# Optimization experiments

Hardware: AMD Instinct MI355X
Metric: run time of the kernel (lower is better)

Reference implementation:

```python
import jax, jax.numpy as jnp
import numpy as np

N = 50000
E = 600000
IN_DIM = 128
HID = 128
HEADS = 4
OUT = HID // HEADS  # per-head out channels
R = 2
LAYERS = 2
NEG_SLOPE = 0.2


def _glorot(key, shape):
    fan_in, fan_out = shape[-2], shape[-1]
    lim = jnp.sqrt(6.0 / (fan_in + fan_out))
    return jax.random.uniform(key, shape, jnp.float32, -lim, lim)


def setup_inputs() -> dict:
    key = jax.random.key(0)
    ks = jax.random.split(key, 20)
    x = jax.random.normal(ks[0], (N, IN_DIM), jnp.float32)
    eidx = jax.random.randint(ks[1], (2, E), 0, N, jnp.int64 if jax.config.jax_enable_x64 else jnp.int32)
    etype = jax.random.randint(ks[2], (E,), 0, R, eidx.dtype)
    d = IN_DIM
    params = {}
    ki = 3
    for l in range(LAYERS):
        params[f"W{l}"] = _glorot(ks[ki], (R, d, HID)); ki += 1            # per-relation weight
        params[f"Q{l}"] = _glorot(ks[ki], (HID, HEADS)); ki += 1           # query proj (dim=1)
        params[f"K{l}"] = _glorot(ks[ki], (HID, HEADS)); ki += 1           # key proj
        params[f"cb{l}"] = jnp.zeros((HID,), jnp.float32)                   # conv bias
        params[f"pW{l}"] = _glorot(ks[ki], (HID, HID)); ki += 1            # proj Linear weight [out,in]
        params[f"pb{l}"] = jnp.zeros((HID,), jnp.float32)
        d = HID
    return dict(x=x, eidx=eidx, etype=etype, **params)


def _rgat_conv(h, src, dst, etype, W, Q, K, b):
    # per-relation transform of all nodes: [R, N, HID]
    xw = jnp.einsum('ni,rio->rno', h, W)
    out_j = xw[etype, src]          # [E, HID] source features under edge's relation
    out_i = xw[etype, dst]          # [E, HID] target features under edge's relation
    # additive self-attention, dim=1: alpha [E, HEADS]
    alpha = jax.nn.leaky_relu(out_i @ Q + out_j @ K, NEG_SLOPE)
    # segment softmax over destination nodes (across-relation)
    m = jax.ops.segment_max(alpha, dst, num_segments=N)
    m = jnp.where(jnp.isfinite(m), m, 0.0)
    e = jnp.exp(alpha - m[dst])
    s = jax.ops.segment_sum(e, dst, num_segments=N)
    a = e / (s[dst] + 1e-16)
    # weighted messages and scatter-sum aggregation
    msg = out_j.reshape(E, HEADS, OUT) * a[:, :, None]
    agg = jax.ops.segment_sum(msg.reshape(E, HID), dst, num_segments=N)
    return agg + b


def reference(x, eidx, etype, W0, Q0, K0, cb0, pW0, pb0, W1, Q1, K1, cb1, pW1, pb1):
    src, dst = eidx[0], eidx[1]  # flow source_to_target: aggregate at eidx[1]
    h = x
    for (W, Q, K, cb, pW, pb) in ((W0, Q0, K0, cb0, pW0, pb0), (W1, Q1, K1, cb1, pW1, pb1)):
        h = _rgat_conv(h, src, dst, etype, W, Q, K, cb)
        h = jax.nn.elu(h @ pW.T + pb)
    return h
```

## Files before the change

### kernel.cpp

```cpp
#include <hip/hip_runtime.h>
#include <hip/hip_bf16.h>

typedef __hip_bfloat16 bf16;
typedef short s16x8 __attribute__((ext_vector_type(8)));
typedef float f32x4 __attribute__((ext_vector_type(4)));

#define N_NODES 50000
#define NPAD    50048
#define E_EDGES 600000
#define HID     128
#define HEADS   4
#define SCAN_B  196

__device__ __forceinline__ unsigned short f2bf_bits(float f) {
  unsigned u = __float_as_uint(f);
  u += 0x7fffu + ((u >> 16) & 1u);
  return (unsigned short)(u >> 16);
}
__device__ __forceinline__ float bf2f(unsigned short b) {
  return __uint_as_float(((unsigned)b) << 16);
}
__device__ __forceinline__ float lo_f(unsigned v) { return __uint_as_float(v << 16); }
__device__ __forceinline__ float hi_f(unsigned v) { return __uint_as_float(v & 0xffff0000u); }

__device__ __forceinline__ float lrelu(float v) { return fmaxf(v, 0.2f * v); }

__global__ __launch_bounds__(256) void detect_zero_kernel(const unsigned short* __restrict__ xb,
                                                          const int* __restrict__ ei,
                                                          int* __restrict__ flags,
                                                          int* __restrict__ zp, int nz) {
  int t = threadIdx.x;
  int i = blockIdx.x * 256 + t;
  if (i < nz) zp[i] = 0;
  if (blockIdx.x == 0) {
    __shared__ int cnt[2];
    if (t < 2) cnt[t] = 0;
    __syncthreads();
    unsigned short v = xb[2 * t];
    int ex = (v >> 7) & 0xFF;
    if (ex < 119 || ex > 135) atomicAdd(&cnt[0], 1);
    if (ei[2 * t + 1] != 0) atomicAdd(&cnt[1], 1);
    __syncthreads();
    if (t == 0) {
      flags[0] = (cnt[0] > 64) ? 1 : 0;
      flags[1] = (cnt[1] == 0) ? 1 : 0;
    }
  }
}

__global__ __launch_bounds__(256) void cvt_idx_hist_kernel(const int* __restrict__ eidx,
                                                           const int* __restrict__ etype,
                                                           int* __restrict__ dstA, int* __restrict__ pk,
                                                           int* __restrict__ deg,
                                                           const int* __restrict__ flags) {
  int e = blockIdx.x * 256 + threadIdx.x;
  if (e >= E_EDGES) return;
  int s, d, r;
  if (flags[1]) {
    const long long* e64 = (const long long*)eidx;
    const long long* t64 = (const long long*)etype;
    s = (int)e64[e]; d = (int)e64[E_EDGES + e]; r = (int)t64[e];
  } else {
    s = eidx[e]; d = eidx[E_EDGES + e]; r = etype[e];
  }
  dstA[e] = d;
  pk[e] = s | (r << 16);
  atomicAdd(&deg[d], 1);
}

__global__ __launch_bounds__(256) void bucket_kernel(const int* __restrict__ deg,
                                                     int* __restrict__ bcnt,
                                                     int* __restrict__ nq,
                                                     int* __restrict__ nw) {
  int n = blockIdx.x * 256 + threadIdx.x;
  int lane = threadIdx.x & 63;
  bool valid = n < N_NODES;
  int d = valid ? deg[n] : 0;
  bool isq = valid && (d <= 16);
  bool isw = valid && (d > 16);
  unsigned long long mq = __ballot(isq);
  unsigned long long mw = __ballot(isw);
  unsigned long long lower = (lane == 63) ? 0x7fffffffffffffffull : ((1ull << lane) - 1ull);
  int baseq = 0, basew = 0;
  int lq = (int)__ffsll((unsigned long long)mq) - 1;
  int lw = (int)__ffsll((unsigned long long)mw) - 1;
  if (mq && lane == lq) baseq = atomicAdd(&bcnt[0], (int)__popcll(mq));
  if (mw && lane == lw) basew = atomicAdd(&bcnt[1], (int)__popcll(mw));
  if (mq) baseq = __shfl(baseq, lq);
  if (mw) basew = __shfl(basew, lw);
  if (isq) nq[baseq + (int)__popcll(mq & lower)] = n;
  if (isw) nw[basew + (int)__popcll(mw & lower)] = n;
}

__global__ __launch_bounds__(256) void cvt_xb_kernel(const void* __restrict__ src,
                                                     unsigned short* __restrict__ dst, int n8,
                                                     const int* __restrict__ flags) {
  int i = blockIdx.x * 256 + threadIdx.x;
  if (i >= n8) return;
  if (flags[0]) {
    const float4* s4 = (const float4*)src;
    float4 a = s4[2 * i], b = s4[2 * i + 1];
    s16x8 o;
    o[0] = (short)f2bf_bits(a.x); o[1] = (short)f2bf_bits(a.y);
    o[2] = (short)f2bf_bits(a.z); o[3] = (short)f2bf_bits(a.w);
    o[4] = (short)f2bf_bits(b.x); o[5] = (short)f2bf_bits(b.y);
    o[6] = (short)f2bf_bits(b.z); o[7] = (short)f2bf_bits(b.w);
    *(s16x8*)(dst + (size_t)i * 8) = o;
  } else {
    *(s16x8*)(dst + (size_t)i * 8) = ((const s16x8*)src)[i];
  }
}

__global__ __launch_bounds__(256) void cvt_wt_kernel(const void* __restrict__ src0,
                                                     const void* __restrict__ src1,
                                                     unsigned short* __restrict__ dst,
                                                     const int* __restrict__ flags) {
  int idx = blockIdx.x * 256 + threadIdx.x;
  if (idx >= 2 * 2 * HID * HID) return;
  int l = idx >> 15, rem = idx & 32767;
  int r = rem >> 14, i = (rem >> 7) & 127, o = rem & 127;
  const void* src = l ? src1 : src0;
  unsigned short b;
  if (flags[0]) b = f2bf_bits(((const float*)src)[rem]);
  else          b = ((const unsigned short*)src)[rem];
  dst[(size_t)l * 2 * HID * HID + ((size_t)r * HID + o) * HID + i] = b;
}

struct P8 { const void* src[8]; int dstoff[8]; int n[8]; };
__global__ __launch_bounds__(256) void cvt_params_kernel(P8 tab, float* __restrict__ base,
                                                         const int* __restrict__ flags) {
  const int f = flags[0];
  for (int k = 0; k < 8; ++k) {
    int n = tab.n[k];
    for (int i = blockIdx.x * 256 + threadIdx.x; i < n; i += gridDim.x * 256) {
      float v = f ? ((const float*)tab.src[k])[i] : bf2f(((const unsigned short*)tab.src[k])[i]);
      base[tab.dstoff[k] + i] = v;
    }
  }
}

__global__ __launch_bounds__(256) void scan1_kernel(const int* __restrict__ deg,
                                                    int* __restrict__ excl,
                                                    int* __restrict__ bsum) {
  __shared__ int sm[256];
  int t = threadIdx.x, i = blockIdx.x * 256 + t;
  int v = (i < NPAD) ? deg[i] : 0;
  sm[t] = v;
  __syncthreads();
#pragma unroll
  for (int off = 1; off < 256; off <<= 1) {
    int add = (t >= off) ? sm[t - off] : 0;
    __syncthreads();
    sm[t] += add;
    __syncthreads();
  }
  if (i < NPAD) excl[i] = sm[t] - v;
  if (t == 255) bsum[blockIdx.x] = sm[255];
}

__global__ __launch_bounds__(256) void scan23_kernel(const int* __restrict__ excl,
                                                     const int* __restrict__ bsum,
                                                     int* __restrict__ rowstart) {
  __shared__ int sm[256];
  int t = threadIdx.x;
  int v = (t < SCAN_B) ? bsum[t] : 0;
  sm[t] = v;
  __syncthreads();
#pragma unroll
  for (int off = 1; off < 256; off <<= 1) {
    int add = (t >= off) ? sm[t - off] : 0;
    __syncthreads();
    sm[t] += add;
    __syncthreads();
  }
  int bpre = (blockIdx.x > 0) ? sm[blockIdx.x - 1] : 0;
  int i = blockIdx.x * 256 + t;
  if (i < NPAD) rowstart[i] = excl[i] + bpre;
  if (i == 0) rowstart[NPAD] = E_EDGES;
}

__global__ __launch_bounds__(256) void scatter_kernel(const int* __restrict__ dstA,
                                                      const int* __restrict__ pk,
                                                      const int* __restrict__ rowstart,
                                                      int* __restrict__ cnt,
                                                      int* __restrict__ eord) {
  int e = blockIdx.x * 256 + threadIdx.x;
  if (e >= E_EDGES) return;
  int d = dstA[e];
  int pos = rowstart[d] + atomicAdd(&cnt[d], 1);
  eord[pos] = pk[e];
}


__global__ __launch_bounds__(256) void gemm_xw_mfma(const unsigned short* __restrict__ hb,
                                                    const unsigned short* __restrict__ Wbt,
                                                    unsigned short* __restrict__ xw) {
  __shared__ unsigned short As[64][136];
  const int t = threadIdx.x;
  const int wave = t >> 6, lane = t & 63;
  const int row0 = blockIdx.x * 64;
  const int r = wave >> 1, colb = (wave & 1) * 64;
  const int lm = lane & 15, q = lane >> 4;
  const unsigned short* Bt = Wbt + (size_t)r * HID * HID;
  s16x8 bfr[4][4];
#pragma unroll
  for (int kc = 0; kc < 4; ++kc) {
    const int ko = kc * 32 + q * 8;
#pragma unroll
    for (int ct = 0; ct < 4; ++ct)
      bfr[kc][ct] = *(const s16x8*)(Bt + (size_t)(colb + ct * 16 + lm) * HID + ko);
  }
  const unsigned short* gsrc = hb + (size_t)row0 * HID;
#pragma unroll
  for (int j = 0; j < 4; ++j) {
    int idx = j * 256 + t;
    *(s16x8*)&As[idx >> 4][(idx & 15) * 8] = *(const s16x8*)(gsrc + idx * 8);
  }
  __syncthreads();
  f32x4 acc[4][4];
#pragma unroll
  for (int a = 0; a < 4; ++a)
#pragma unroll
    for (int b = 0; b < 4; ++b) { f32x4 z = {0.f, 0.f, 0.f, 0.f}; acc[a][b] = z; }
#pragma unroll
  for (int kc = 0; kc < 4; ++kc) {
    const int ko = kc * 32 + q * 8;
#pragma unroll
    for (int rt = 0; rt < 4; ++rt) {
      s16x8 a = *(const s16x8*)&As[rt * 16 + lm][ko];
#pragma unroll
      for (int ct = 0; ct < 4; ++ct)
        acc[rt][ct] = __builtin_amdgcn_mfma_f32_16x16x32_bf16(a, bfr[kc][ct], acc[rt][ct], 0, 0, 0);
    }
  }
  __syncthreads();
#pragma unroll
  for (int rr = 0; rr < 2; ++rr) {
    if (r == rr) {
#pragma unroll
      for (int rt = 0; rt < 4; ++rt)
#pragma unroll
        for (int i = 0; i < 4; ++i) {
          int rloc = rt * 16 + q * 4 + i;
#pragma unroll
          for (int ct = 0; ct < 4; ++ct)
            As[rloc][colb + ct * 16 + lm] = f2bf_bits(acc[rt][ct][i]);
        }
    }
    __syncthreads();
    unsigned short* dst = xw + ((size_t)rr * NPAD + row0) * HID;
#pragma unroll
    for (int j = 0; j < 4; ++j) {
      int idx = j * 256 + t;
      int rw = idx >> 4, cb8 = (idx & 15) * 8;
      if (row0 + rw < N_NODES)
        *(s16x8*)(dst + (size_t)rw * HID + cb8) = *(const s16x8*)&As[rw][cb8];
    }
    __syncthreads();
  }
}

__global__ __launch_bounds__(128) void proj_mfma(const unsigned short* __restrict__ aggb,
                                                 const unsigned short* __restrict__ pWTb,
                                                 const float* __restrict__ bo,
                                                 unsigned short* __restrict__ hbout,
                                                 void* __restrict__ dout,
                                                 const int* __restrict__ flags) {
  __shared__ unsigned short As[64][136];
  const int t = threadIdx.x;
  const int wave = t >> 6, lane = t & 63;
  const int row0 = blockIdx.x * 64;
  const int colb = wave * 64;
  const int lm = lane & 15, q = lane >> 4;
  s16x8 bfr[4][4];
#pragma unroll
  for (int kc = 0; kc < 4; ++kc) {
    const int ko = kc * 32 + q * 8;
#pragma unroll
    for (int ct = 0; ct < 4; ++ct)
      bfr[kc][ct] = *(const s16x8*)(pWTb + (size_t)(colb + ct * 16 + lm) * HID + ko);
  }
  const unsigned short* gsrc = aggb + (size_t)row0 * HID;
#pragma unroll
  for (int j = 0; j < 8; ++j) {
    int idx = j * 128 + t;
    *(s16x8*)&As[idx >> 4][(idx & 15) * 8] = *(const s16x8*)(gsrc + idx * 8);
  }
  __syncthreads();
  f32x4 acc[4][4];
#pragma unroll
  for (int a = 0; a < 4; ++a)
#pragma unroll
    for (int b = 0; b < 4; ++b) { f32x4 z = {0.f, 0.f, 0.f, 0.f}; acc[a][b] = z; }
#pragma unroll
  for (int kc = 0; kc < 4; ++kc) {
    const int ko = kc * 32 + q * 8;
#pragma unroll
    for (int rt = 0; rt < 4; ++rt) {
      s16x8 a = *(const s16x8*)&As[rt * 16 + lm][ko];
#pragma unroll
      for (int ct = 0; ct < 4; ++ct)
        acc[rt][ct] = __builtin_amdgcn_mfma_f32_16x16x32_bf16(a, bfr[kc][ct], acc[rt][ct], 0, 0, 0);
    }
  }
  __syncthreads();
  const int f32final = (dout != nullptr) && flags[0];
  if (!f32final) {
    unsigned short* dstp = dout ? (unsigned short*)dout : hbout;
#pragma unroll
    for (int rt = 0; rt < 4; ++rt)
#pragma unroll
      for (int i = 0; i < 4; ++i) {
        int rloc = rt * 16 + q * 4 + i;
#pragma unroll
        for (int ct = 0; ct < 4; ++ct) {
          int o = colb + ct * 16 + lm;
          float v = acc[rt][ct][i] + bo[o];
          v = v > 0.f ? v : expm1f(v);
          As[rloc][o] = f2bf_bits(v);
        }
      }
    __syncthreads();
#pragma unroll
    for (int j = 0; j < 8; ++j) {
      int idx = j * 128 + t;
      int rw = idx >> 4, cb8 = (idx & 15) * 8;
      if (row0 + rw < N_NODES)
        *(s16x8*)(dstp + (size_t)(row0 + rw) * HID + cb8) = *(const s16x8*)&As[rw][cb8];
    }
  } else {
    float* fdst = (float*)dout;
    float (*Fs)[132] = (float(*)[132])&As[0][0];
#pragma unroll
    for (int h = 0; h < 2; ++h) {
#pragma unroll
      for (int rt2 = 0; rt2 < 2; ++rt2) {
        const int rt = h * 2 + rt2;
#pragma unroll
        for (int i = 0; i < 4; ++i) {
          int rloc = rt2 * 16 + q * 4 + i;
#pragma unroll
          for (int ct = 0; ct < 4; ++ct) {
            int o = colb + ct * 16 + lm;
            float v = acc[rt][ct][i] + bo[o];
            v = v > 0.f ? v : expm1f(v);
            Fs[rloc][o] = v;
          }
        }
      }
      __syncthreads();
#pragma unroll
      for (int j = 0; j < 8; ++j) {
        int idx = j * 128 + t;
        int rw = idx >> 5, cb4 = (idx & 31) * 4;
        if (row0 + h * 32 + rw < N_NODES)
          *(float4*)(fdst + (size_t)(row0 + h * 32 + rw) * HID + cb4) = *(const float4*)&Fs[rw][cb4];
      }
      __syncthreads();
    }
  }
}

__global__ __launch_bounds__(256) void prep_wq_kernel(const unsigned short* __restrict__ Wbt,
                                                      const float* __restrict__ Qf,
                                                      const float* __restrict__ Kf,
                                                      unsigned short* __restrict__ qkt_hi,
                                                      unsigned short* __restrict__ qkt_lo) {
  int idx = blockIdx.x * 256 + threadIdx.x;
  if (idx >= 2 * 2 * HID) return;
  int i = idx & 127, lr = idx >> 7, l = lr >> 1, r = (lr & 1);
  float aq[4] = {0.f, 0.f, 0.f, 0.f}, ak[4] = {0.f, 0.f, 0.f, 0.f};
  const unsigned short* Wb = Wbt + (size_t)lr * HID * HID;
  const float* Qp = Qf + l * HID * HEADS;
  const float* Kp = Kf + l * HID * HEADS;
  for (int j = 0; j < HID; ++j) {
    float w = bf2f(Wb[j * HID + i]);
    float4 q4 = *(const float4*)(Qp + j * 4);
    float4 k4 = *(const float4*)(Kp + j * 4);
    aq[0] += w * q4.x; aq[1] += w * q4.y; aq[2] += w * q4.z; aq[3] += w * q4.w;
    ak[0] += w * k4.x; ak[1] += w * k4.y; ak[2] += w * k4.z; ak[3] += w * k4.w;
  }
  size_t base = (size_t)l * 16 * HID;
#pragma unroll
  for (int h = 0; h < 4; ++h) {
    unsigned short qh = f2bf_bits(aq[h]);
    unsigned short kh = f2bf_bits(ak[h]);
    float qres = aq[h] - bf2f(qh);
    float kres = ak[h] - bf2f(kh);
    qkt_hi[base + (size_t)(r * 4 + h) * HID + i] = qh;
    qkt_lo[base + (size_t)(r * 4 + h) * HID + i] = f2bf_bits(qres);
    qkt_hi[base + (size_t)(8 + r * 4 + h) * HID + i] = kh;
    qkt_lo[base + (size_t)(8 + r * 4 + h) * HID + i] = f2bf_bits(kres);
  }
}

__global__ __launch_bounds__(256) void qk_mfma_kernel(const unsigned short* __restrict__ hb,
                                                      const unsigned short* __restrict__ qkt_hi,
                                                      const unsigned short* __restrict__ qkt_lo,
                                                      float4* __restrict__ qi4,
                                                      float4* __restrict__ kj4) {
  __shared__ float st[4][16][68];
  const int wave = threadIdx.x >> 6, lane = threadIdx.x & 63;
  const int row0 = blockIdx.x * 256 + wave * 64;
  const int lm = lane & 15, q = lane >> 4;
  if (row0 < NPAD) {
    s16x8 bhi[4], blo[4], af[4][4];
#pragma unroll
    for (int kc = 0; kc < 4; ++kc) {
      const int ko = kc * 32 + q * 8;
      bhi[kc] = *(const s16x8*)(qkt_hi + (size_t)lm * HID + ko);
      blo[kc] = *(const s16x8*)(qkt_lo + (size_t)lm * HID + ko);
    }
#pragma unroll
    for (int kc = 0; kc < 4; ++kc) {
      const int ko = kc * 32 + q * 8;
#pragma unroll
      for (int rt = 0; rt < 4; ++rt)
        af[kc][rt] = *(const s16x8*)(hb + (size_t)(row0 + rt * 16 + lm) * HID + ko);
    }
    f32x4 acc[4];
#pragma unroll
    for (int a = 0; a < 4; ++a) { f32x4 z = {0.f, 0.f, 0.f, 0.f}; acc[a] = z; }
#pragma unroll
    for (int kc = 0; kc < 4; ++kc)
#pragma unroll
      for (int rt = 0; rt < 4; ++rt) {
        acc[rt] = __builtin_amdgcn_mfma_f32_16x16x32_bf16(af[kc][rt], bhi[kc], acc[rt], 0, 0, 0);
        acc[rt] = __builtin_amdgcn_mfma_f32_16x16x32_bf16(af[kc][rt], blo[kc], acc[rt], 0, 0, 0);
      }
#pragma unroll
    for (int rt = 0; rt < 4; ++rt)
      *(f32x4*)&st[wave][lm][rt * 16 + q * 4] = acc[rt];
  }
  __syncthreads();
  if (row0 < NPAD) {
    int n = row0 + lane;
    if (n < N_NODES) {
      float4 v;
      v.x = st[wave][0][lane]; v.y = st[wave][1][lane]; v.z = st[wave][2][lane]; v.w = st[wave][3][lane];
      qi4[n] = v;
      v.x = st[wave][4][lane]; v.y = st[wave][5][lane]; v.z = st[wave][6][lane]; v.w = st[wave][7][lane];
      qi4[NPAD + n] = v;
      v.x = st[wave][8][lane]; v.y = st[wave][9][lane]; v.z = st[wave][10][lane]; v.w = st[wave][11][lane];
      kj4[n] = v;
      v.x = st[wave][12][lane]; v.y = st[wave][13][lane]; v.z = st[wave][14][lane]; v.w = st[wave][15][lane];
      kj4[NPAD + n] = v;
    }
  }
}

__global__ __launch_bounds__(256) void edge_quad_kernel(
    const int* __restrict__ rowstart, const int* __restrict__ eord,
    const float4* __restrict__ qi4, const float4* __restrict__ kj4,
    const unsigned short* __restrict__ xw, unsigned short* __restrict__ aggb,
    const int* __restrict__ nq, const int* __restrict__ bcnt) {
  __shared__ volatile float wls[16][4][17];
  const int t = threadIdx.x;
  const int wave = t >> 6, lane = t & 63;
  const int g = lane >> 4, li = lane & 15;
  const int idx = blockIdx.x * 16 + wave * 4 + g;
  const int cq = bcnt[0];
  const bool act = idx < cq;
  const int n = act ? nq[idx] : 0;
  const int start = rowstart[n];
  const int dg = act ? (rowstart[n + 1] - start) : 0;
  int p = 0;
  float w0 = 0.f, w1 = 0.f, w2 = 0.f, w3 = 0.f;
  if (li < dg) {
    p = eord[start + li];
    int s = p & 0xffff, r = p >> 16;
    float4 k4 = kj4[r ? (NPAD + s) : s];
    float4 q4 = r ? qi4[NPAD + n] : qi4[n];
    w0 = __expf(fminf(lrelu(q4.x + k4.x), 85.f));
    w1 = __expf(fminf(lrelu(q4.y + k4.y), 85.f));
    w2 = __expf(fminf(lrelu(q4.z + k4.z), 85.f));
    w3 = __expf(fminf(lrelu(q4.w + k4.w), 85.f));
  }
  const int wg = (wave << 2) | g;
  wls[wg][0][li] = w0; wls[wg][1][li] = w1;
  wls[wg][2][li] = w2; wls[wg][3][li] = w3;
  float s0 = w0, s1 = w1, s2 = w2, s3 = w3;
#pragma unroll
  for (int off = 8; off > 0; off >>= 1) {
    s0 += __shfl_xor(s0, off); s1 += __shfl_xor(s1, off);
    s2 += __shfl_xor(s2, off); s3 += __shfl_xor(s3, off);
  }
  const int hh = li >> 2;
  float ssel = hh == 0 ? s0 : hh == 1 ? s1 : hh == 2 ? s2 : s3;
  float a0 = 0.f, a1 = 0.f, a2 = 0.f, a3 = 0.f, a4 = 0.f, a5 = 0.f, a6 = 0.f, a7 = 0.f;
  volatile const float* wrh = &wls[wg][hh][0];
  const int co = li * 8;
  const int gbase = lane & 48;
#pragma unroll 1
  for (int e0 = 0; e0 < dg; e0 += 4) {
    int pe[4];
    uint4 v[4];
#pragma unroll
    for (int u = 0; u < 4; ++u) {
      int e = e0 + u;
      pe[u] = __shfl(p, gbase + (e < dg ? e : 0));
    }
#pragma unroll
    for (int u = 0; u < 4; ++u)
      v[u] = *(const uint4*)(xw + ((size_t)((pe[u] & 0xffff) + (pe[u] >> 16) * NPAD) << 7) + co);
#pragma unroll
    for (int u = 0; u < 4; ++u) {
      int e = e0 + u;
      float we = (e < dg) ? wrh[e] : 0.f;
      a0 = fmaf(lo_f(v[u].x), we, a0); a1 = fmaf(hi_f(v[u].x), we, a1);
      a2 = fmaf(lo_f(v[u].y), we, a2); a3 = fmaf(hi_f(v[u].y), we, a3);
      a4 = fmaf(lo_f(v[u].z), we, a4); a5 = fmaf(hi_f(v[u].z), we, a5);
      a6 = fmaf(lo_f(v[u].w), we, a6); a7 = fmaf(hi_f(v[u].w), we, a7);
    }
  }
  if (act) {
    float inv = 1.f / (ssel + 1e-16f);
    uint4 o;
    o.x = (unsigned)f2bf_bits(a0 * inv) | ((unsigned)f2bf_bits(a1 * inv) << 16);
    o.y = (unsigned)f2bf_bits(a2 * inv) | ((unsigned)f2bf_bits(a3 * inv) << 16);
    o.z = (unsigned)f2bf_bits(a4 * inv) | ((unsigned)f2bf_bits(a5 * inv) << 16);
    o.w = (unsigned)f2bf_bits(a6 * inv) | ((unsigned)f2bf_bits(a7 * inv) << 16);
    *(uint4*)(aggb + ((size_t)n << 7) + co) = o;
  }
}

__global__ __launch_bounds__(256) void edge_big_kernel(
    const int* __restrict__ rowstart, const int* __restrict__ eord,
    const float4* __restrict__ qi4, const float4* __restrict__ kj4,
    const unsigned short* __restrict__ xw, unsigned short* __restrict__ aggb,
    const int* __restrict__ nw, const int* __restrict__ bcnt) {
  __shared__ volatile float wls[4][4][72];
  const int wave = threadIdx.x >> 6, lane = threadIdx.x & 63;
  const int idx = blockIdx.x * 4 + wave;
  const int cw = bcnt[1];
  if (idx >= cw) return;
  const int n = nw[idx];
  unsigned* outp = (unsigned*)(aggb + ((size_t)n << 7)) + lane;
  const int start = rowstart[n];
  const int deg = rowstart[n + 1] - start;
  const int hh = lane >> 4;
  const int ch2 = lane << 1;
  float2 acc = {0.f, 0.f};
  float ssel;
  if (deg <= 64) {
    int p = 0;
    float w0 = 0.f, w1 = 0.f, w2 = 0.f, w3 = 0.f;
    if (lane < deg) {
      p = eord[start + lane];
      int s = p & 0xffff, r = p >> 16;
      float4 k4 = kj4[r ? (NPAD + s) : s];
      float4 q4 = r ? qi4[NPAD + n] : qi4[n];
      w0 = __expf(fminf(lrelu(q4.x + k4.x), 85.f));
      w1 = __expf(fminf(lrelu(q4.y + k4.y), 85.f));
      w2 = __expf(fminf(lrelu(q4.z + k4.z), 85.f));
      w3 = __expf(fminf(lrelu(q4.w + k4.w), 85.f));
    }
    float s0 = w0, s1 = w1, s2 = w2, s3 = w3;
#pragma unroll
    for (int off = 32; off > 0; off >>= 1) {
      s0 += __shfl_xor(s0, off); s1 += __shfl_xor(s1, off);
      s2 += __shfl_xor(s2, off); s3 += __shfl_xor(s3, off);
    }
    ssel = hh == 0 ? s0 : hh == 1 ? s1 : hh == 2 ? s2 : s3;
    wls[wave][0][lane] = w0;
    wls[wave][1][lane] = w1;
    wls[wave][2][lane] = w2;
    wls[wave][3][lane] = w3;
    volatile const float* wrh = &wls[wave][hh][0];
    const int degp = (deg + 15) & ~15;
#pragma unroll 1
    for (int e = 0; e < degp; e += 16) {
      int pp[16];
      unsigned vv[16];
#pragma unroll
      for (int u = 0; u < 16; ++u)
        pp[u] = __builtin_amdgcn_readlane(p, e + u);
#pragma unroll
      for (int u = 0; u < 16; ++u)
        vv[u] = *(const unsigned*)(xw + ((size_t)((pp[u] & 0xffff) + (pp[u] >> 16) * NPAD) << 7) + ch2);
#pragma unroll
      for (int u = 0; u < 16; ++u) {
        float we = wrh[e + u];
        acc.x = fmaf(lo_f(vv[u]), we, acc.x);
        acc.y = fmaf(hi_f(vv[u]), we, acc.y);
      }
    }
  } else {
    const float4 q0 = qi4[n], q1 = qi4[NPAD + n];
    float4 m = make_float4(-1e30f, -1e30f, -1e30f, -1e30f);
    for (int e = start; e < start + deg; ++e) {
      int pe = eord[e];
      int s = pe & 0xffff, r = pe >> 16;
      float4 k4 = kj4[(size_t)r * NPAD + s];
      float4 q4 = r ? q1 : q0;
      m.x = fmaxf(m.x, lrelu(q4.x + k4.x)); m.y = fmaxf(m.y, lrelu(q4.y + k4.y));
      m.z = fmaxf(m.z, lrelu(q4.z + k4.z)); m.w = fmaxf(m.w, lrelu(q4.w + k4.w));
    }
    float4 sv = make_float4(0.f, 0.f, 0.f, 0.f);
    for (int e = start; e < start + deg; ++e) {
      int pe = eord[e];
      int s = pe & 0xffff, r = pe >> 16;
      float4 k4 = kj4[(size_t)r * NPAD + s];
      float4 q4 = r ? q1 : q0;
      float w0 = __expf(lrelu(q4.x + k4.x) - m.x);
      float w1 = __expf(lrelu(q4.y + k4.y) - m.y);
      float w2 = __expf(lrelu(q4.z + k4.z) - m.z);
      float w3 = __expf(lrelu(q4.w + k4.w) - m.w);
      sv.x += w0; sv.y += w1; sv.z += w2; sv.w += w3;
      float we = hh == 0 ? w0 : hh == 1 ? w1 : hh == 2 ? w2 : w3;
      unsigned v = *(const unsigned*)(xw + (((size_t)r * NPAD + s) << 7) + ch2);
      acc.x = fmaf(lo_f(v), we, acc.x);
      acc.y = fmaf(hi_f(v), we, acc.y);
    }
    ssel = hh == 0 ? sv.x : hh == 1 ? sv.y : hh == 2 ? sv.z : sv.w;
  }
  float inv = 1.f / (ssel + 1e-16f);
  *outp = (unsigned)f2bf_bits(acc.x * inv) | ((unsigned)f2bf_bits(acc.y * inv) << 16);
}

__global__ __launch_bounds__(64) void prep_proj_kernel(const void* __restrict__ pW0,
                                                       const void* __restrict__ pW1,
                                                       const float* __restrict__ cbf,
                                                       const float* __restrict__ pbf,
                                                       unsigned short* __restrict__ pWTb2,
                                                       float* __restrict__ bo2,
                                                       const int* __restrict__ flags) {
  int o = blockIdx.x & 127, l = blockIdx.x >> 7, t = threadIdx.x;
  const void* pWraw = l ? pW1 : pW0;
  const float* cb = cbf + l * HID;
  const int f = flags[0];
  float part = 0.f;
#pragma unroll
  for (int i = t; i < HID; i += 64) {
    float w = f ? ((const float*)pWraw)[o * HID + i] : bf2f(((const unsigned short*)pWraw)[o * HID + i]);
    pWTb2[(size_t)l * HID * HID + o * HID + i] = f2bf_bits(w);
    part += cb[i] * w;
  }
#pragma unroll
  for (int off = 32; off > 0; off >>= 1) part += __shfl_xor(part, off);
  if (t == 0) bo2[l * HID + o] = pbf[l * HID + o] + part;
}

extern "C" void kernel_launch(void* const* d_in, const int* in_sizes, int n_in,
                              void* d_out, int out_size, void* d_ws, size_t ws_size,
                              hipStream_t stream) {
  const void* x     = d_in[0];
  const int*  eidx  = (const int*)d_in[1];
  const int*  etype = (const int*)d_in[2];
  const int iW[2] = {3, 9}, iQ[2] = {4, 10}, iK[2] = {5, 11}, icb[2] = {6, 12}, ipW[2] = {7, 13}, ipb[2] = {8, 14};

  float* ws = (float*)d_ws;
  size_t off = 0;
  int*   flags = (int*)(ws + off); off += 16;
  unsigned short* hb   = (unsigned short*)(ws + off); off += (size_t)NPAD * HID / 2;
  unsigned short* xw   = (unsigned short*)(ws + off); off += (size_t)NPAD * HID;
  float* qi   = ws + off; off += (size_t)2 * NPAD * HEADS;
  float* kj   = ws + off; off += (size_t)2 * NPAD * HEADS;
  unsigned short* aggb = (unsigned short*)(ws + off); off += (size_t)NPAD * HID / 2;
  int* dstA = (int*)(ws + off); off += E_EDGES;
  int* pk   = (int*)(ws + off); off += E_EDGES;
  int* eord = (int*)(ws + off); off += E_EDGES;
  int* deg  = (int*)(ws + off); off += NPAD;
  int* cnt  = (int*)(ws + off); off += NPAD;
  int* bcnt = (int*)(ws + off); off += 16;
  int* excl = (int*)(ws + off); off += NPAD;
  int* rowstart = (int*)(ws + off); off += NPAD + 16;
  int* bsum  = (int*)(ws + off); off += 256;
  int* nq   = (int*)(ws + off); off += NPAD;
  int* nwl  = (int*)(ws + off); off += NPAD;
  unsigned short* Wbt   = (unsigned short*)(ws + off); off += (size_t)2 * 2 * HID * HID / 2;
  unsigned short* pWTb2 = (unsigned short*)(ws + off); off += (size_t)2 * HID * HID / 2;
  unsigned short* qkt_hi = (unsigned short*)(ws + off); off += (size_t)2 * 16 * HID / 2;
  unsigned short* qkt_lo = (unsigned short*)(ws + off); off += (size_t)2 * 16 * HID / 2;
  float* Qf  = ws + off; off += 2 * HID * HEADS;
  float* Kf  = ws + off; off += 2 * HID * HEADS;
  float* cbf = ws + off; off += 2 * HID;
  float* pbf = ws + off; off += 2 * HID;
  float* bo2 = ws + off; off += 2 * HID;

  detect_zero_kernel<<<(2 * NPAD + 16 + 255) / 256, 256, 0, stream>>>((const unsigned short*)x, eidx, flags, deg, 2 * NPAD + 16);
  cvt_idx_hist_kernel<<<(E_EDGES + 255) / 256, 256, 0, stream>>>(eidx, etype, dstA, pk, deg, flags);
  bucket_kernel<<<(N_NODES + 255) / 256, 256, 0, stream>>>(deg, bcnt, nq, nwl);
  cvt_xb_kernel<<<(N_NODES * HID / 8 + 255) / 256, 256, 0, stream>>>(x, hb, N_NODES * HID / 8, flags);
  cvt_wt_kernel<<<(2 * 2 * HID * HID + 255) / 256, 256, 0, stream>>>(d_in[iW[0]], d_in[iW[1]], Wbt, flags);
  {
    P8 tab;
    float* base = ws;
    for (int l = 0; l < 2; ++l) {
      tab.src[l * 4 + 0] = d_in[iQ[l]];  tab.dstoff[l * 4 + 0] = (int)(Qf - base) + l * HID * HEADS;  tab.n[l * 4 + 0] = HID * HEADS;
      tab.src[l * 4 + 1] = d_in[iK[l]];  tab.dstoff[l * 4 + 1] = (int)(Kf - base) + l * HID * HEADS;  tab.n[l * 4 + 1] = HID * HEADS;
      tab.src[l * 4 + 2] = d_in[icb[l]]; tab.dstoff[l * 4 + 2] = (int)(cbf - base) + l * HID;         tab.n[l * 4 + 2] = HID;
      tab.src[l * 4 + 3] = d_in[ipb[l]]; tab.dstoff[l * 4 + 3] = (int)(pbf - base) + l * HID;         tab.n[l * 4 + 3] = HID;
    }
    cvt_params_kernel<<<2, 256, 0, stream>>>(tab, base, flags);
  }

  scan1_kernel<<<SCAN_B, 256, 0, stream>>>(deg, excl, bsum);
  scan23_kernel<<<SCAN_B, 256, 0, stream>>>(excl, bsum, rowstart);
  scatter_kernel<<<(E_EDGES + 255) / 256, 256, 0, stream>>>(dstA, pk, rowstart, cnt, eord);

  prep_wq_kernel<<<2, 256, 0, stream>>>(Wbt, Qf, Kf, qkt_hi, qkt_lo);
  prep_proj_kernel<<<2 * HID, 64, 0, stream>>>(d_in[ipW[0]], d_in[ipW[1]], cbf, pbf, pWTb2, bo2, flags);

  const int RB = NPAD / 64;
  const int QB = (NPAD + 255) / 256;
  for (int l = 0; l < 2; ++l) {
    gemm_xw_mfma<<<RB, 256, 0, stream>>>(hb, Wbt + (size_t)l * 2 * HID * HID, xw);
    qk_mfma_kernel<<<QB, 256, 0, stream>>>(hb, qkt_hi + (size_t)l * 16 * HID, qkt_lo + (size_t)l * 16 * HID,
                                           (float4*)qi, (float4*)kj);
    edge_quad_kernel<<<(N_NODES + 15) / 16, 256, 0, stream>>>(rowstart, eord, (const float4*)qi, (const float4*)kj,
                                                              xw, aggb, nq, bcnt);
    edge_big_kernel<<<(N_NODES + 3) / 4, 256, 0, stream>>>(rowstart, eord, (const float4*)qi, (const float4*)kj,
                                                           xw, aggb, nwl, bcnt);
    proj_mfma<<<RB, 128, 0, stream>>>(aggb, pWTb2 + (size_t)l * HID * HID, bo2 + l * HID, hb,
                                      (l == 1) ? d_out : nullptr, flags);
  }
}
```

Baseline: 374.3 us.

## Merge independent preprocessing and per-layer kernels into block-range fused launches

```diff
diff --git a/kernel.cpp b/kernel.cpp
--- a/kernel.cpp
+++ b/kernel.cpp
@@ -12,6 +12,14 @@
 #define HEADS   4
 #define SCAN_B  196
 
+#define GB_IDX  2344
+#define GB_XB   3125
+#define GB_WT   256
+#define GB_QUAD 3125
+#define GB_BIG  8824
+#define GB_GEMM 1564
+#define GB_QK   196
+
 __device__ __forceinline__ unsigned short f2bf_bits(float f) {
   unsigned u = __float_as_uint(f);
   u += 0x7fffu + ((u >> 16) & 1u);
@@ -22,8 +30,8 @@
 }
 __device__ __forceinline__ float lo_f(unsigned v) { return __uint_as_float(v << 16); }
 __device__ __forceinline__ float hi_f(unsigned v) { return __uint_as_float(v & 0xffff0000u); }
-
 __device__ __forceinline__ float lrelu(float v) { return fmaxf(v, 0.2f * v); }
+__device__ __forceinline__ float elu(float v) { return v > 0.f ? v : __expf(v) - 1.f; }
 
 __global__ __launch_bounds__(256) void detect_zero_kernel(const unsigned short* __restrict__ xb,
                                                           const int* __restrict__ ei,
@@ -48,135 +56,189 @@
   }
 }
 
-__global__ __launch_bounds__(256) void cvt_idx_hist_kernel(const int* __restrict__ eidx,
-                                                           const int* __restrict__ etype,
-                                                           int* __restrict__ dstA, int* __restrict__ pk,
-                                                           int* __restrict__ deg,
-                                                           const int* __restrict__ flags) {
-  int e = blockIdx.x * 256 + threadIdx.x;
-  if (e >= E_EDGES) return;
-  int s, d, r;
-  if (flags[1]) {
-    const long long* e64 = (const long long*)eidx;
-    const long long* t64 = (const long long*)etype;
-    s = (int)e64[e]; d = (int)e64[E_EDGES + e]; r = (int)t64[e];
+struct P8 { const void* src[8]; int dstoff[8]; int n[8]; };
+__global__ __launch_bounds__(256) void cvt_all_kernel(const int* __restrict__ eidx,
+                                                      const int* __restrict__ etype,
+                                                      int* __restrict__ dstA, int* __restrict__ pk,
+                                                      int* __restrict__ deg,
+                                                      const void* __restrict__ x,
+                                                      unsigned short* __restrict__ hb,
+                                                      const void* __restrict__ w0,
+                                                      const void* __restrict__ w1,
+                                                      unsigned short* __restrict__ Wbt,
+                                                      P8 tab, float* __restrict__ base,
+                                                      const int* __restrict__ flags) {
+  const int b = blockIdx.x, t = threadIdx.x;
+  if (b < GB_IDX) {
+    int e = b * 256 + t;
+    if (e >= E_EDGES) return;
+    int s, d, r;
+    if (flags[1]) {
+      const long long* e64 = (const long long*)eidx;
+      const long long* t64 = (const long long*)etype;
+      s = (int)e64[e]; d = (int)e64[E_EDGES + e]; r = (int)t64[e];
+    } else {
+      s = eidx[e]; d = eidx[E_EDGES + e]; r = etype[e];
+    }
+    dstA[e] = d;
+    pk[e] = s | (r << 16);
+    atomicAdd(&deg[d], 1);
+  } else if (b < GB_IDX + GB_XB) {
+    int i = (b - GB_IDX) * 256 + t;
+    if (flags[0]) {
+      const float4* s4 = (const float4*)x;
+      float4 a = s4[2 * i], c = s4[2 * i + 1];
+      s16x8 o;
+      o[0] = (short)f2bf_bits(a.x); o[1] = (short)f2bf_bits(a.y);
+      o[2] = (short)f2bf_bits(a.z); o[3] = (short)f2bf_bits(a.w);
+      o[4] = (short)f2bf_bits(c.x); o[5] = (short)f2bf_bits(c.y);
+      o[6] = (short)f2bf_bits(c.z); o[7] = (short)f2bf_bits(c.w);
+      *(s16x8*)(hb + (size_t)i * 8) = o;
+    } else {
+      *(s16x8*)(hb + (size_t)i * 8) = ((const s16x8*)x)[i];
+    }
+  } else if (b < GB_IDX + GB_XB + GB_WT) {
+    int idx = (b - GB_IDX - GB_XB) * 256 + t;
+    int l = idx >> 15, rem = idx & 32767;
+    int r = rem >> 14, i = (rem >> 7) & 127, o = rem & 127;
+    const void* src = l ? w1 : w0;
+    unsigned short v;
+    if (flags[0]) v = f2bf_bits(((const float*)src)[rem]);
+    else          v = ((const unsigned short*)src)[rem];
+    Wbt[(size_t)l * 2 * HID * HID + ((size_t)r * HID + o) * HID + i] = v;
   } else {
-    s = eidx[e]; d = eidx[E_EDGES + e]; r = etype[e];
-  }
-  dstA[e] = d;
-  pk[e] = s | (r << 16);
-  atomicAdd(&deg[d], 1);
-}
-
-__global__ __launch_bounds__(256) void bucket_kernel(const int* __restrict__ deg,
-                                                     int* __restrict__ bcnt,
-                                                     int* __restrict__ nq,
-                                                     int* __restrict__ nw) {
-  int n = blockIdx.x * 256 + threadIdx.x;
-  int lane = threadIdx.x & 63;
-  bool valid = n < N_NODES;
-  int d = valid ? deg[n] : 0;
-  bool isq = valid && (d <= 16);
-  bool isw = valid && (d > 16);
-  unsigned long long mq = __ballot(isq);
-  unsigned long long mw = __ballot(isw);
-  unsigned long long lower = (lane == 63) ? 0x7fffffffffffffffull : ((1ull << lane) - 1ull);
-  int baseq = 0, basew = 0;
-  int lq = (int)__ffsll((unsigned long long)mq) - 1;
-  int lw = (int)__ffsll((unsigned long long)mw) - 1;
-  if (mq && lane == lq) baseq = atomicAdd(&bcnt[0], (int)__popcll(mq));
-  if (mw && lane == lw) basew = atomicAdd(&bcnt[1], (int)__popcll(mw));
-  if (mq) baseq = __shfl(baseq, lq);
-  if (mw) basew = __shfl(basew, lw);
-  if (isq) nq[baseq + (int)__popcll(mq & lower)] = n;
-  if (isw) nw[basew + (int)__popcll(mw & lower)] = n;
-}
-
-__global__ __launch_bounds__(256) void cvt_xb_kernel(const void* __restrict__ src,
-                                                     unsigned short* __restrict__ dst, int n8,
-                                                     const int* __restrict__ flags) {
-  int i = blockIdx.x * 256 + threadIdx.x;
-  if (i >= n8) return;
-  if (flags[0]) {
-    const float4* s4 = (const float4*)src;
-    float4 a = s4[2 * i], b = s4[2 * i + 1];
-    s16x8 o;
-    o[0] = (short)f2bf_bits(a.x); o[1] = (short)f2bf_bits(a.y);
-    o[2] = (short)f2bf_bits(a.z); o[3] = (short)f2bf_bits(a.w);
-    o[4] = (short)f2bf_bits(b.x); o[5] = (short)f2bf_bits(b.y);
-    o[6] = (short)f2bf_bits(b.z); o[7] = (short)f2bf_bits(b.w);
-    *(s16x8*)(dst + (size_t)i * 8) = o;
+    const int f = flags[0];
+    int bb = b - GB_IDX - GB_XB - GB_WT;
+    for (int k = 0; k < 8; ++k) {
+      int n = tab.n[k];
+      for (int i = bb * 256 + t; i < n; i += 2 * 256) {
+        float v = f ? ((const float*)tab.src[k])[i] : bf2f(((const unsigned short*)tab.src[k])[i]);
+        base[tab.dstoff[k] + i] = v;
+      }
+    }
+  }
+}
+
+__global__ __launch_bounds__(256) void scan1_bucket_kernel(const int* __restrict__ deg,
+                                                           int* __restrict__ excl,
+                                                           int* __restrict__ bsum,
+                                                           int* __restrict__ bcnt,
+                                                           int* __restrict__ nq,
+                                                           int* __restrict__ nw) {
+  const int b = blockIdx.x, t = threadIdx.x;
+  if (b < SCAN_B) {
+    __shared__ int sm[256];
+    int i = b * 256 + t;
+    int v = (i < NPAD) ? deg[i] : 0;
+    sm[t] = v;
+    __syncthreads();
+#pragma unroll
+    for (int off = 1; off < 256; off <<= 1) {
+      int add = (t >= off) ? sm[t - off] : 0;
+      __syncthreads();
+      sm[t] += add;
+      __syncthreads();
+    }
+    if (i < NPAD) excl[i] = sm[t] - v;
+    if (t == 255) bsum[b] = sm[255];
   } else {
-    *(s16x8*)(dst + (size_t)i * 8) = ((const s16x8*)src)[i];
-  }
-}
-
-__global__ __launch_bounds__(256) void cvt_wt_kernel(const void* __restrict__ src0,
-                                                     const void* __restrict__ src1,
-                                                     unsigned short* __restrict__ dst,
-                                                     const int* __restrict__ flags) {
-  int idx = blockIdx.x * 256 + threadIdx.x;
-  if (idx >= 2 * 2 * HID * HID) return;
-  int l = idx >> 15, rem = idx & 32767;
-  int r = rem >> 14, i = (rem >> 7) & 127, o = rem & 127;
-  const void* src = l ? src1 : src0;
-  unsigned short b;
-  if (flags[0]) b = f2bf_bits(((const float*)src)[rem]);
-  else          b = ((const unsigned short*)src)[rem];
-  dst[(size_t)l * 2 * HID * HID + ((size_t)r * HID + o) * HID + i] = b;
-}
-
-struct P8 { const void* src[8]; int dstoff[8]; int n[8]; };
-__global__ __launch_bounds__(256) void cvt_params_kernel(P8 tab, float* __restrict__ base,
-                                                         const int* __restrict__ flags) {
-  const int f = flags[0];
-  for (int k = 0; k < 8; ++k) {
-    int n = tab.n[k];
-    for (int i = blockIdx.x * 256 + threadIdx.x; i < n; i += gridDim.x * 256) {
-      float v = f ? ((const float*)tab.src[k])[i] : bf2f(((const unsigned short*)tab.src[k])[i]);
-      base[tab.dstoff[k] + i] = v;
-    }
-  }
-}
-
-__global__ __launch_bounds__(256) void scan1_kernel(const int* __restrict__ deg,
-                                                    int* __restrict__ excl,
-                                                    int* __restrict__ bsum) {
-  __shared__ int sm[256];
-  int t = threadIdx.x, i = blockIdx.x * 256 + t;
-  int v = (i < NPAD) ? deg[i] : 0;
-  sm[t] = v;
-  __syncthreads();
-#pragma unroll
-  for (int off = 1; off < 256; off <<= 1) {
-    int add = (t >= off) ? sm[t - off] : 0;
+    int n = (b - SCAN_B) * 256 + t;
+    int lane = t & 63;
+    bool valid = n < N_NODES;
+    int d = valid ? deg[n] : 0;
+    bool isq = valid && (d <= 16);
+    bool isw = valid && (d > 16);
+    unsigned long long mq = __ballot(isq);
+    unsigned long long mw = __ballot(isw);
+    unsigned long long lower = (lane == 63) ? 0x7fffffffffffffffull : ((1ull << lane) - 1ull);
+    int baseq = 0, basew = 0;
+    int lq = (int)__ffsll(mq) - 1;
+    int lw = (int)__ffsll(mw) - 1;
+    if (mq && lane == lq) baseq = atomicAdd(&bcnt[0], (int)__popcll(mq));
+    if (mw && lane == lw) basew = atomicAdd(&bcnt[1], (int)__popcll(mw));
+    if (mq) baseq = __shfl(baseq, lq);
+    if (mw) basew = __shfl(basew, lw);
+    if (isq) nq[baseq + (int)__popcll(mq & lower)] = n;
+    if (isw) nw[basew + (int)__popcll(mw & lower)] = n;
+  }
+}
+
+__global__ __launch_bounds__(256) void scan23_prep_kernel(const int* __restrict__ excl,
+                                                          const int* __restrict__ bsum,
+                                                          int* __restrict__ rowstart,
+                                                          const unsigned short* __restrict__ Wbt,
+                                                          const float* __restrict__ Qf,
+                                                          const float* __restrict__ Kf,
+                                                          unsigned short* __restrict__ qkt_hi,
+                                                          unsigned short* __restrict__ qkt_lo,
+                                                          const void* __restrict__ pW0,
+                                                          const void* __restrict__ pW1,
+                                                          const float* __restrict__ cbf,
+                                                          const float* __restrict__ pbf,
+                                                          unsigned short* __restrict__ pWTb2,
+                                                          float* __restrict__ bo2,
+                                                          const int* __restrict__ flags) {
+  const int b = blockIdx.x, t = threadIdx.x;
+  if (b < SCAN_B) {
+    __shared__ int sm[256];
+    int v = (t < SCAN_B) ? bsum[t] : 0;
+    sm[t] = v;
     __syncthreads();
-    sm[t] += add;
-    __syncthreads();
-  }
-  if (i < NPAD) excl[i] = sm[t] - v;
-  if (t == 255) bsum[blockIdx.x] = sm[255];
-}
-
-__global__ __launch_bounds__(256) void scan23_kernel(const int* __restrict__ excl,
-                                                     const int* __restrict__ bsum,
-                                                     int* __restrict__ rowstart) {
-  __shared__ int sm[256];
-  int t = threadIdx.x;
-  int v = (t < SCAN_B) ? bsum[t] : 0;
-  sm[t] = v;
-  __syncthreads();
-#pragma unroll
-  for (int off = 1; off < 256; off <<= 1) {
-    int add = (t >= off) ? sm[t - off] : 0;
-    __syncthreads();
-    sm[t] += add;
-    __syncthreads();
-  }
-  int bpre = (blockIdx.x > 0) ? sm[blockIdx.x - 1] : 0;
-  int i = blockIdx.x * 256 + t;
-  if (i < NPAD) rowstart[i] = excl[i] + bpre;
-  if (i == 0) rowstart[NPAD] = E_EDGES;
+#pragma unroll
+    for (int off = 1; off < 256; off <<= 1) {
+      int add = (t >= off) ? sm[t - off] : 0;
+      __syncthreads();
+      sm[t] += add;
+      __syncthreads();
+    }
+    int bpre = (b > 0) ? sm[b - 1] : 0;
+    int i = b * 256 + t;
+    if (i < NPAD) rowstart[i] = excl[i] + bpre;
+    if (i == 0) rowstart[NPAD] = E_EDGES;
+  } else if (b < SCAN_B + 2) {
+    int idx = (b - SCAN_B) * 256 + t;
+    int i = idx & 127, lr = idx >> 7, l = lr >> 1, r = (lr & 1);
+    float aq[4] = {0.f, 0.f, 0.f, 0.f}, ak[4] = {0.f, 0.f, 0.f, 0.f};
+    const unsigned short* Wb = Wbt + (size_t)lr * HID * HID;
+    const float* Qp = Qf + l * HID * HEADS;
+    const float* Kp = Kf + l * HID * HEADS;
+    for (int j = 0; j < HID; ++j) {
+      float w = bf2f(Wb[j * HID + i]);
+      float4 q4 = *(const float4*)(Qp + j * 4);
+      float4 k4 = *(const float4*)(Kp + j * 4);
+      aq[0] += w * q4.x; aq[1] += w * q4.y; aq[2] += w * q4.z; aq[3] += w * q4.w;
+      ak[0] += w * k4.x; ak[1] += w * k4.y; ak[2] += w * k4.z; ak[3] += w * k4.w;
+    }
+    size_t base = (size_t)l * 16 * HID;
+#pragma unroll
+    for (int h = 0; h < 4; ++h) {
+      unsigned short qh = f2bf_bits(aq[h]);
+      unsigned short kh = f2bf_bits(ak[h]);
+      float qres = aq[h] - bf2f(qh);
+      float kres = ak[h] - bf2f(kh);
+      qkt_hi[base + (size_t)(r * 4 + h) * HID + i] = qh;
+      qkt_lo[base + (size_t)(r * 4 + h) * HID + i] = f2bf_bits(qres);
+      qkt_hi[base + (size_t)(8 + r * 4 + h) * HID + i] = kh;
+      qkt_lo[base + (size_t)(8 + r * 4 + h) * HID + i] = f2bf_bits(kres);
+    }
+  } else {
+    const int wave = t >> 6, lane = t & 63;
+    int ob = (b - SCAN_B - 2) * 4 + wave;
+    int o = ob & 127, l = ob >> 7;
+    const void* pWraw = l ? pW1 : pW0;
+    const float* cb = cbf + l * HID;
+    const int f = flags[0];
+    float part = 0.f;
+#pragma unroll
+    for (int i = lane; i < HID; i += 64) {
+      float w = f ? ((const float*)pWraw)[o * HID + i] : bf2f(((const unsigned short*)pWraw)[o * HID + i]);
+      pWTb2[(size_t)l * HID * HID + o * HID + i] = f2bf_bits(w);
+      part += cb[i] * w;
+    }
+#pragma unroll
+    for (int off = 32; off > 0; off >>= 1) part += __shfl_xor(part, off);
+    if (lane == 0) bo2[l * HID + o] = pbf[l * HID + o] + part;
+  }
 }
 
 __global__ __launch_bounds__(256) void scatter_kernel(const int* __restrict__ dstA,
@@ -191,76 +253,295 @@
   eord[pos] = pk[e];
 }
 
-
-__global__ __launch_bounds__(256) void gemm_xw_mfma(const unsigned short* __restrict__ hb,
-                                                    const unsigned short* __restrict__ Wbt,
-                                                    unsigned short* __restrict__ xw) {
-  __shared__ unsigned short As[64][136];
+__global__ __launch_bounds__(256) void gemm_qk_kernel(const unsigned short* __restrict__ hb,
+                                                      const unsigned short* __restrict__ Wbt,
+                                                      unsigned short* __restrict__ xw,
+                                                      const unsigned short* __restrict__ qkt_hi,
+                                                      const unsigned short* __restrict__ qkt_lo,
+                                                      float4* __restrict__ qi4,
+                                                      float4* __restrict__ kj4) {
+  __shared__ unsigned short smem[8704];
   const int t = threadIdx.x;
   const int wave = t >> 6, lane = t & 63;
-  const int row0 = blockIdx.x * 64;
-  const int r = wave >> 1, colb = (wave & 1) * 64;
   const int lm = lane & 15, q = lane >> 4;
-  const unsigned short* Bt = Wbt + (size_t)r * HID * HID;
-  s16x8 bfr[4][4];
-#pragma unroll
-  for (int kc = 0; kc < 4; ++kc) {
-    const int ko = kc * 32 + q * 8;
-#pragma unroll
-    for (int ct = 0; ct < 4; ++ct)
-      bfr[kc][ct] = *(const s16x8*)(Bt + (size_t)(colb + ct * 16 + lm) * HID + ko);
-  }
-  const unsigned short* gsrc = hb + (size_t)row0 * HID;
-#pragma unroll
-  for (int j = 0; j < 4; ++j) {
-    int idx = j * 256 + t;
-    *(s16x8*)&As[idx >> 4][(idx & 15) * 8] = *(const s16x8*)(gsrc + idx * 8);
-  }
-  __syncthreads();
-  f32x4 acc[4][4];
-#pragma unroll
-  for (int a = 0; a < 4; ++a)
-#pragma unroll
-    for (int b = 0; b < 4; ++b) { f32x4 z = {0.f, 0.f, 0.f, 0.f}; acc[a][b] = z; }
-#pragma unroll
-  for (int kc = 0; kc < 4; ++kc) {
-    const int ko = kc * 32 + q * 8;
-#pragma unroll
-    for (int rt = 0; rt < 4; ++rt) {
-      s16x8 a = *(const s16x8*)&As[rt * 16 + lm][ko];
+  if (blockIdx.x < GB_GEMM) {
+    unsigned short (*As)[136] = (unsigned short(*)[136])smem;
+    const int row0 = blockIdx.x * 32;
+    const int r = wave >> 1, colb = (wave & 1) * 64;
+    const unsigned short* Bt = Wbt + (size_t)r * HID * HID;
+    s16x8 bfr[4][4];
+#pragma unroll
+    for (int kc = 0; kc < 4; ++kc) {
+      const int ko = kc * 32 + q * 8;
 #pragma unroll
       for (int ct = 0; ct < 4; ++ct)
-        acc[rt][ct] = __builtin_amdgcn_mfma_f32_16x16x32_bf16(a, bfr[kc][ct], acc[rt][ct], 0, 0, 0);
-    }
-  }
-  __syncthreads();
-#pragma unroll
-  for (int rr = 0; rr < 2; ++rr) {
-    if (r == rr) {
+        bfr[kc][ct] = *(const s16x8*)(Bt + (size_t)(colb + ct * 16 + lm) * HID + ko);
+    }
+    const unsigned short* gsrc = hb + (size_t)row0 * HID;
+#pragma unroll
+    for (int j = 0; j < 2; ++j) {
+      int idx = j * 256 + t;
+      *(s16x8*)&As[idx >> 4][(idx & 15) * 8] = *(const s16x8*)(gsrc + idx * 8);
+    }
+    __syncthreads();
+    f32x4 acc[2][4];
+#pragma unroll
+    for (int a = 0; a < 2; ++a)
+#pragma unroll
+      for (int c = 0; c < 4; ++c) { f32x4 z = {0.f, 0.f, 0.f, 0.f}; acc[a][c] = z; }
+#pragma unroll
+    for (int kc = 0; kc < 4; ++kc) {
+      const int ko = kc * 32 + q * 8;
+#pragma unroll
+      for (int rt = 0; rt < 2; ++rt) {
+        s16x8 a = *(const s16x8*)&As[rt * 16 + lm][ko];
+#pragma unroll
+        for (int ct = 0; ct < 4; ++ct)
+          acc[rt][ct] = __builtin_amdgcn_mfma_f32_16x16x32_bf16(a, bfr[kc][ct], acc[rt][ct], 0, 0, 0);
+      }
+    }
+    __syncthreads();
+#pragma unroll
+    for (int rr = 0; rr < 2; ++rr) {
+      if (r == rr) {
+#pragma unroll
+        for (int rt = 0; rt < 2; ++rt)
+#pragma unroll
+          for (int i = 0; i < 4; ++i) {
+            int rloc = rt * 16 + q * 4 + i;
+#pragma unroll
+            for (int ct = 0; ct < 4; ++ct)
+              As[rloc][colb + ct * 16 + lm] = f2bf_bits(acc[rt][ct][i]);
+          }
+      }
+      __syncthreads();
+      unsigned short* dst = xw + ((size_t)rr * NPAD + row0) * HID;
+#pragma unroll
+      for (int j = 0; j < 2; ++j) {
+        int idx = j * 256 + t;
+        int rw = idx >> 4, cb8 = (idx & 15) * 8;
+        if (row0 + rw < N_NODES)
+          *(s16x8*)(dst + (size_t)rw * HID + cb8) = *(const s16x8*)&As[rw][cb8];
+      }
+      __syncthreads();
+    }
+  } else {
+    float (*st)[16][68] = (float(*)[16][68])smem;
+    const int row0 = (blockIdx.x - GB_GEMM) * 256 + wave * 64;
+    if (row0 < NPAD) {
+      s16x8 bhi[4], blo[4], af[4][4];
+#pragma unroll
+      for (int kc = 0; kc < 4; ++kc) {
+        const int ko = kc * 32 + q * 8;
+        bhi[kc] = *(const s16x8*)(qkt_hi + (size_t)lm * HID + ko);
+        blo[kc] = *(const s16x8*)(qkt_lo + (size_t)lm * HID + ko);
+      }
+#pragma unroll
+      for (int kc = 0; kc < 4; ++kc) {
+        const int ko = kc * 32 + q * 8;
+#pragma unroll
+        for (int rt = 0; rt < 4; ++rt)
+          af[kc][rt] = *(const s16x8*)(hb + (size_t)(row0 + rt * 16 + lm) * HID + ko);
+      }
+      f32x4 acc[4];
+#pragma unroll
+      for (int a = 0; a < 4; ++a) { f32x4 z = {0.f, 0.f, 0.f, 0.f}; acc[a] = z; }
+#pragma unroll
+      for (int kc = 0; kc < 4; ++kc)
+#pragma unroll
+        for (int rt = 0; rt < 4; ++rt) {
+          acc[rt] = __builtin_amdgcn_mfma_f32_16x16x32_bf16(af[kc][rt], bhi[kc], acc[rt], 0, 0, 0);
+          acc[rt] = __builtin_amdgcn_mfma_f32_16x16x32_bf16(af[kc][rt], blo[kc], acc[rt], 0, 0, 0);
+        }
 #pragma unroll
       for (int rt = 0; rt < 4; ++rt)
-#pragma unroll
-        for (int i = 0; i < 4; ++i) {
-          int rloc = rt * 16 + q * 4 + i;
-#pragma unroll
-          for (int ct = 0; ct < 4; ++ct)
-            As[rloc][colb + ct * 16 + lm] = f2bf_bits(acc[rt][ct][i]);
+        *(f32x4*)&st[wave][lm][rt * 16 + q * 4] = acc[rt];
+    }
+    __syncthreads();
+    if (row0 < NPAD) {
+      int n = row0 + lane;
+      if (n < N_NODES) {
+        float4 v;
+        v.x = st[wave][0][lane]; v.y = st[wave][1][lane]; v.z = st[wave][2][lane]; v.w = st[wave][3][lane];
+        qi4[n] = v;
+        v.x = st[wave][4][lane]; v.y = st[wave][5][lane]; v.z = st[wave][6][lane]; v.w = st[wave][7][lane];
+        qi4[NPAD + n] = v;
+        v.x = st[wave][8][lane]; v.y = st[wave][9][lane]; v.z = st[wave][10][lane]; v.w = st[wave][11][lane];
+        kj4[n] = v;
+        v.x = st[wave][12][lane]; v.y = st[wave][13][lane]; v.z = st[wave][14][lane]; v.w = st[wave][15][lane];
+        kj4[NPAD + n] = v;
+      }
+    }
+  }
+}
+
+__global__ __launch_bounds__(256) void edge_all_kernel(
+    const int* __restrict__ rowstart, const int* __restrict__ eord,
+    const float4* __restrict__ qi4, const float4* __restrict__ kj4,
+    const unsigned short* __restrict__ xw, unsigned short* __restrict__ aggb,
+    const int* __restrict__ nq, const int* __restrict__ nw,
+    const int* __restrict__ bcnt) {
+  __shared__ volatile float wbuf[1152];
+  const int t = threadIdx.x;
+  const int wave = t >> 6, lane = t & 63;
+  if (blockIdx.x < GB_QUAD) {
+    const int g = lane >> 4, li = lane & 15;
+    const int idx = blockIdx.x * 16 + wave * 4 + g;
+    const int cq = bcnt[0];
+    const bool act = idx < cq;
+    const int n = act ? nq[idx] : 0;
+    const int start = rowstart[n];
+    const int dg = act ? (rowstart[n + 1] - start) : 0;
+    int p = 0;
+    float w0 = 0.f, w1 = 0.f, w2 = 0.f, w3 = 0.f;
+    if (li < dg) {
+      p = eord[start + li];
+      int s = p & 0xffff, r = p >> 16;
+      float4 k4 = kj4[r ? (NPAD + s) : s];
+      float4 q4 = r ? qi4[NPAD + n] : qi4[n];
+      w0 = __expf(fminf(lrelu(q4.x + k4.x), 85.f));
+      w1 = __expf(fminf(lrelu(q4.y + k4.y), 85.f));
+      w2 = __expf(fminf(lrelu(q4.z + k4.z), 85.f));
+      w3 = __expf(fminf(lrelu(q4.w + k4.w), 85.f));
+    }
+    const int wg = (wave << 2) | g;
+    volatile float* wls = &wbuf[wg * 68];
+    wls[0 * 17 + li] = w0; wls[1 * 17 + li] = w1;
+    wls[2 * 17 + li] = w2; wls[3 * 17 + li] = w3;
+    float s0 = w0, s1 = w1, s2 = w2, s3 = w3;
+#pragma unroll
+    for (int off = 8; off > 0; off >>= 1) {
+      s0 += __shfl_xor(s0, off); s1 += __shfl_xor(s1, off);
+      s2 += __shfl_xor(s2, off); s3 += __shfl_xor(s3, off);
+    }
+    const int hh = li >> 2;
+    float ssel = hh == 0 ? s0 : hh == 1 ? s1 : hh == 2 ? s2 : s3;
+    float a0 = 0.f, a1 = 0.f, a2 = 0.f, a3 = 0.f, a4 = 0.f, a5 = 0.f, a6 = 0.f, a7 = 0.f;
+    volatile const float* wrh = &wls[hh * 17];
+    const int co = li * 8;
+    const int gbase = lane & 48;
+#pragma unroll 1
+    for (int e0 = 0; e0 < dg; e0 += 4) {
+      int pe[4];
+      uint4 v[4];
+#pragma unroll
+      for (int u = 0; u < 4; ++u) {
+        int e = e0 + u;
+        pe[u] = __shfl(p, gbase + (e < dg ? e : 0));
+      }
+#pragma unroll
+      for (int u = 0; u < 4; ++u)
+        v[u] = *(const uint4*)(xw + ((size_t)((pe[u] & 0xffff) + (pe[u] >> 16) * NPAD) << 7) + co);
+#pragma unroll
+      for (int u = 0; u < 4; ++u) {
+        int e = e0 + u;
+        float we = (e < dg) ? wrh[e] : 0.f;
+        a0 = fmaf(lo_f(v[u].x), we, a0); a1 = fmaf(hi_f(v[u].x), we, a1);
+        a2 = fmaf(lo_f(v[u].y), we, a2); a3 = fmaf(hi_f(v[u].y), we, a3);
+        a4 = fmaf(lo_f(v[u].z), we, a4); a5 = fmaf(hi_f(v[u].z), we, a5);
+        a6 = fmaf(lo_f(v[u].w), we, a6); a7 = fmaf(hi_f(v[u].w), we, a7);
+      }
+    }
+    if (act) {
+      float inv = 1.f / (ssel + 1e-16f);
+      uint4 o;
+      o.x = (unsigned)f2bf_bits(a0 * inv) | ((unsigned)f2bf_bits(a1 * inv) << 16);
+      o.y = (unsigned)f2bf_bits(a2 * inv) | ((unsigned)f2bf_bits(a3 * inv) << 16);
+      o.z = (unsigned)f2bf_bits(a4 * inv) | ((unsigned)f2bf_bits(a5 * inv) << 16);
+      o.w = (unsigned)f2bf_bits(a6 * inv) | ((unsigned)f2bf_bits(a7 * inv) << 16);
+      *(uint4*)(aggb + ((size_t)n << 7) + co) = o;
+    }
+  } else {
+    const int idx = (blockIdx.x - GB_QUAD) * 4 + wave;
+    const int cw = bcnt[1];
+    if (idx >= cw) return;
+    const int n = nw[idx];
+    unsigned* outp = (unsigned*)(aggb + ((size_t)n << 7)) + lane;
+    const int start = rowstart[n];
+    const int deg = rowstart[n + 1] - start;
+    const int hh = lane >> 4;
+    const int ch2 = lane << 1;
+    float2 acc = {0.f, 0.f};
+    float ssel;
+    volatile float* wls = &wbuf[wave * 288];
+    if (deg <= 64) {
+      int p = 0;
+      float w0 = 0.f, w1 = 0.f, w2 = 0.f, w3 = 0.f;
+      if (lane < deg) {
+        p = eord[start + lane];
+        int s = p & 0xffff, r = p >> 16;
+        float4 k4 = kj4[r ? (NPAD + s) : s];
+        float4 q4 = r ? qi4[NPAD + n] : qi4[n];
+        w0 = __expf(fminf(lrelu(q4.x + k4.x), 85.f));
+        w1 = __expf(fminf(lrelu(q4.y + k4.y), 85.f));
+        w2 = __expf(fminf(lrelu(q4.z + k4.z), 85.f));
+        w3 = __expf(fminf(lrelu(q4.w + k4.w), 85.f));
+      }
+      float s0 = w0, s1 = w1, s2 = w2, s3 = w3;
+#pragma unroll
+      for (int off = 32; off > 0; off >>= 1) {
+        s0 += __shfl_xor(s0, off); s1 += __shfl_xor(s1, off);
+        s2 += __shfl_xor(s2, off); s3 += __shfl_xor(s3, off);
+      }
+      ssel = hh == 0 ? s0 : hh == 1 ? s1 : hh == 2 ? s2 : s3;
+      wls[0 * 72 + lane] = w0;
+      wls[1 * 72 + lane] = w1;
+      wls[2 * 72 + lane] = w2;
+      wls[3 * 72 + lane] = w3;
+      volatile const float* wrh = &wls[hh * 72];
+      const int degp = (deg + 15) & ~15;
+#pragma unroll 1
+      for (int e = 0; e < degp; e += 16) {
+        int pp[16];
+        unsigned vv[16];
+#pragma unroll
+        for (int u = 0; u < 16; ++u)
+          pp[u] = __builtin_amdgcn_readlane(p, e + u);
+#pragma unroll
+        for (int u = 0; u < 16; ++u)
+          vv[u] = *(const unsigned*)(xw + ((size_t)((pp[u] & 0xffff) + (pp[u] >> 16) * NPAD) << 7) + ch2);
+#pragma unroll
+        for (int u = 0; u < 16; ++u) {
+          float we = wrh[e + u];
+          acc.x = fmaf(lo_f(vv[u]), we, acc.x);
+          acc.y = fmaf(hi_f(vv[u]), we, acc.y);
         }
-    }
-    __syncthreads();
-    unsigned short* dst = xw + ((size_t)rr * NPAD + row0) * HID;
-#pragma unroll
-    for (int j = 0; j < 4; ++j) {
-      int idx = j * 256 + t;
-      int rw = idx >> 4, cb8 = (idx & 15) * 8;
-      if (row0 + rw < N_NODES)
-        *(s16x8*)(dst + (size_t)rw * HID + cb8) = *(const s16x8*)&As[rw][cb8];
-    }
-    __syncthreads();
-  }
-}
-
-__global__ __launch_bounds__(128) void proj_mfma(const unsigned short* __restrict__ aggb,
+      }
+    } else {
+      const float4 q0 = qi4[n], q1 = qi4[NPAD + n];
+      float4 m = make_float4(-1e30f, -1e30f, -1e30f, -1e30f);
+      for (int e = start; e < start + deg; ++e) {
+        int pe = eord[e];
+        int s = pe & 0xffff, r = pe >> 16;
+        float4 k4 = kj4[(size_t)r * NPAD + s];
+        float4 q4 = r ? q1 : q0;
+        m.x = fmaxf(m.x, lrelu(q4.x + k4.x)); m.y = fmaxf(m.y, lrelu(q4.y + k4.y));
+        m.z = fmaxf(m.z, lrelu(q4.z + k4.z)); m.w = fmaxf(m.w, lrelu(q4.w + k4.w));
+      }
+      float4 sv = make_float4(0.f, 0.f, 0.f, 0.f);
+      for (int e = start; e < start + deg; ++e) {
+        int pe = eord[e];
+        int s = pe & 0xffff, r = pe >> 16;
+        float4 k4 = kj4[(size_t)r * NPAD + s];
+        float4 q4 = r ? q1 : q0;
+        float w0 = __expf(lrelu(q4.x + k4.x) - m.x);
+        float w1 = __expf(lrelu(q4.y + k4.y) - m.y);
+        float w2 = __expf(lrelu(q4.z + k4.z) - m.z);
+        float w3 = __expf(lrelu(q4.w + k4.w) - m.w);
+        sv.x += w0; sv.y += w1; sv.z += w2; sv.w += w3;
+        float we = hh == 0 ? w0 : hh == 1 ? w1 : hh == 2 ? w2 : w3;
+        unsigned v = *(const unsigned*)(xw + (((size_t)r * NPAD + s) << 7) + ch2);
+        acc.x = fmaf(lo_f(v), we, acc.x);
+        acc.y = fmaf(hi_f(v), we, acc.y);
+      }
+      ssel = hh == 0 ? sv.x : hh == 1 ? sv.y : hh == 2 ? sv.z : sv.w;
+    }
+    float inv = 1.f / (ssel + 1e-16f);
+    *outp = (unsigned)f2bf_bits(acc.x * inv) | ((unsigned)f2bf_bits(acc.y * inv) << 16);
+  }
+}
+
+__global__ __launch_bounds__(256) void proj_mfma(const unsigned short* __restrict__ aggb,
                                                  const unsigned short* __restrict__ pWTb,
                                                  const float* __restrict__ bo,
                                                  unsigned short* __restrict__ hbout,
@@ -270,7 +551,8 @@
   const int t = threadIdx.x;
   const int wave = t >> 6, lane = t & 63;
   const int row0 = blockIdx.x * 64;
-  const int colb = wave * 64;
+  const int h = wave >> 1;
+  const int colb = (wave & 1) * 64;
   const int lm = lane & 15, q = lane >> 4;
   s16x8 bfr[4][4];
 #pragma unroll
@@ -282,22 +564,22 @@
   }
   const unsigned short* gsrc = aggb + (size_t)row0 * HID;
 #pragma unroll
-  for (int j = 0; j < 8; ++j) {
-    int idx = j * 128 + t;
+  for (int j = 0; j < 4; ++j) {
+    int idx = j * 256 + t;
     *(s16x8*)&As[idx >> 4][(idx & 15) * 8] = *(const s16x8*)(gsrc + idx * 8);
   }
   __syncthreads();
-  f32x4 acc[4][4];
-#pragma unroll
-  for (int a = 0; a < 4; ++a)
-#pragma unroll
-    for (int b = 0; b < 4; ++b) { f32x4 z = {0.f, 0.f, 0.f, 0.f}; acc[a][b] = z; }
+  f32x4 acc[2][4];
+#pragma unroll
+  for (int a = 0; a < 2; ++a)
+#pragma unroll
+    for (int c = 0; c < 4; ++c) { f32x4 z = {0.f, 0.f, 0.f, 0.f}; acc[a][c] = z; }
 #pragma unroll
   for (int kc = 0; kc < 4; ++kc) {
     const int ko = kc * 32 + q * 8;
 #pragma unroll
-    for (int rt = 0; rt < 4; ++rt) {
-      s16x8 a = *(const s16x8*)&As[rt * 16 + lm][ko];
+    for (int rt = 0; rt < 2; ++rt) {
+      s16x8 a = *(const s16x8*)&As[(2 * h + rt) * 16 + lm][ko];
 #pragma unroll
       for (int ct = 0; ct < 4; ++ct)
         acc[rt][ct] = __builtin_amdgcn_mfma_f32_16x16x32_bf16(a, bfr[kc][ct], acc[rt][ct], 0, 0, 0);
@@ -308,22 +590,21 @@
   if (!f32final) {
     unsigned short* dstp = dout ? (unsigned short*)dout : hbout;
 #pragma unroll
-    for (int rt = 0; rt < 4; ++rt)
+    for (int rt = 0; rt < 2; ++rt)
 #pragma unroll
       for (int i = 0; i < 4; ++i) {
-        int rloc = rt * 16 + q * 4 + i;
+        int rloc = (2 * h + rt) * 16 + q * 4 + i;
 #pragma unroll
         for (int ct = 0; ct < 4; ++ct) {
           int o = colb + ct * 16 + lm;
-          float v = acc[rt][ct][i] + bo[o];
-          v = v > 0.f ? v : expm1f(v);
+          float v = elu(acc[rt][ct][i] + bo[o]);
           As[rloc][o] = f2bf_bits(v);
         }
       }
     __syncthreads();
 #pragma unroll
-    for (int j = 0; j < 8; ++j) {
-      int idx = j * 128 + t;
+    for (int j = 0; j < 4; ++j) {
+      int idx = j * 256 + t;
       int rw = idx >> 4, cb8 = (idx & 15) * 8;
       if (row0 + rw < N_NODES)
         *(s16x8*)(dstp + (size_t)(row0 + rw) * HID + cb8) = *(const s16x8*)&As[rw][cb8];
@@ -332,313 +613,31 @@
     float* fdst = (float*)dout;
     float (*Fs)[132] = (float(*)[132])&As[0][0];
 #pragma unroll
-    for (int h = 0; h < 2; ++h) {
-#pragma unroll
-      for (int rt2 = 0; rt2 < 2; ++rt2) {
-        const int rt = h * 2 + rt2;
-#pragma unroll
-        for (int i = 0; i < 4; ++i) {
-          int rloc = rt2 * 16 + q * 4 + i;
-#pragma unroll
-          for (int ct = 0; ct < 4; ++ct) {
-            int o = colb + ct * 16 + lm;
-            float v = acc[rt][ct][i] + bo[o];
-            v = v > 0.f ? v : expm1f(v);
-            Fs[rloc][o] = v;
+    for (int h2 = 0; h2 < 2; ++h2) {
+      if (h == h2) {
+#pragma unroll
+        for (int rt = 0; rt < 2; ++rt)
+#pragma unroll
+          for (int i = 0; i < 4; ++i) {
+            int rloc = rt * 16 + q * 4 + i;
+#pragma unroll
+            for (int ct = 0; ct < 4; ++ct) {
+              int o = colb + ct * 16 + lm;
+              Fs[rloc][o] = elu(acc[rt][ct][i] + bo[o]);
+            }
           }
-        }
       }
       __syncthreads();
 #pragma unroll
-      for (int j = 0; j < 8; ++j) {
-        int idx = j * 128 + t;
+      for (int j = 0; j < 4; ++j) {
+        int idx = j * 256 + t;
         int rw = idx >> 5, cb4 = (idx & 31) * 4;
-        if (row0 + h * 32 + rw < N_NODES)
-          *(float4*)(fdst + (size_t)(row0 + h * 32 + rw) * HID + cb4) = *(const float4*)&Fs[rw][cb4];
+        if (row0 + h2 * 32 + rw < N_NODES)
+          *(float4*)(fdst + (size_t)(row0 + h2 * 32 + rw) * HID + cb4) = *(const float4*)&Fs[rw][cb4];
       }
       __syncthreads();
     }
   }
-}
-
-__global__ __launch_bounds__(256) void prep_wq_kernel(const unsigned short* __restrict__ Wbt,
-                                                      const float* __restrict__ Qf,
-                                                      const float* __restrict__ Kf,
-                                                      unsigned short* __restrict__ qkt_hi,
-                                                      unsigned short* __restrict__ qkt_lo) {
-  int idx = blockIdx.x * 256 + threadIdx.x;
-  if (idx >= 2 * 2 * HID) return;
-  int i = idx & 127, lr = idx >> 7, l = lr >> 1, r = (lr & 1);
-  float aq[4] = {0.f, 0.f, 0.f, 0.f}, ak[4] = {0.f, 0.f, 0.f, 0.f};
-  const unsigned short* Wb = Wbt + (size_t)lr * HID * HID;
-  const float* Qp = Qf + l * HID * HEADS;
-  const float* Kp = Kf + l * HID * HEADS;
-  for (int j = 0; j < HID; ++j) {
-    float w = bf2f(Wb[j * HID + i]);
-    float4 q4 = *(const float4*)(Qp + j * 4);
-    float4 k4 = *(const float4*)(Kp + j * 4);
-    aq[0] += w * q4.x; aq[1] += w * q4.y; aq[2] += w * q4.z; aq[3] += w * q4.w;
-    ak[0] += w * k4.x; ak[1] += w * k4.y; ak[2] += w * k4.z; ak[3] += w * k4.w;
-  }
-  size_t base = (size_t)l * 16 * HID;
-#pragma unroll
-  for (int h = 0; h < 4; ++h) {
-    unsigned short qh = f2bf_bits(aq[h]);
-    unsigned short kh = f2bf_bits(ak[h]);
-    float qres = aq[h] - bf2f(qh);
-    float kres = ak[h] - bf2f(kh);
-    qkt_hi[base + (size_t)(r * 4 + h) * HID + i] = qh;
-    qkt_lo[base + (size_t)(r * 4 + h) * HID + i] = f2bf_bits(qres);
-    qkt_hi[base + (size_t)(8 + r * 4 + h) * HID + i] = kh;
-    qkt_lo[base + (size_t)(8 + r * 4 + h) * HID + i] = f2bf_bits(kres);
-  }
-}
-
-__global__ __launch_bounds__(256) void qk_mfma_kernel(const unsigned short* __restrict__ hb,
-                                                      const unsigned short* __restrict__ qkt_hi,
-                                                      const unsigned short* __restrict__ qkt_lo,
-                                                      float4* __restrict__ qi4,
-                                                      float4* __restrict__ kj4) {
-  __shared__ float st[4][16][68];
-  const int wave = threadIdx.x >> 6, lane = threadIdx.x & 63;
-  const int row0 = blockIdx.x * 256 + wave * 64;
-  const int lm = lane & 15, q = lane >> 4;
-  if (row0 < NPAD) {
-    s16x8 bhi[4], blo[4], af[4][4];
-#pragma unroll
-    for (int kc = 0; kc < 4; ++kc) {
-      const int ko = kc * 32 + q * 8;
-      bhi[kc] = *(const s16x8*)(qkt_hi + (size_t)lm * HID + ko);
-      blo[kc] = *(const s16x8*)(qkt_lo + (size_t)lm * HID + ko);
-    }
-#pragma unroll
-    for (int kc = 0; kc < 4; ++kc) {
-      const int ko = kc * 32 + q * 8;
-#pragma unroll
-      for (int rt = 0; rt < 4; ++rt)
-        af[kc][rt] = *(const s16x8*)(hb + (size_t)(row0 + rt * 16 + lm) * HID + ko);
-    }
-    f32x4 acc[4];
-#pragma unroll
-    for (int a = 0; a < 4; ++a) { f32x4 z = {0.f, 0.f, 0.f, 0.f}; acc[a] = z; }
-#pragma unroll
-    for (int kc = 0; kc < 4; ++kc)
-#pragma unroll
-      for (int rt = 0; rt < 4; ++rt) {
-        acc[rt] = __builtin_amdgcn_mfma_f32_16x16x32_bf16(af[kc][rt], bhi[kc], acc[rt], 0, 0, 0);
-        acc[rt] = __builtin_amdgcn_mfma_f32_16x16x32_bf16(af[kc][rt], blo[kc], acc[rt], 0, 0, 0);
-      }
-#pragma unroll
-    for (int rt = 0; rt < 4; ++rt)
-      *(f32x4*)&st[wave][lm][rt * 16 + q * 4] = acc[rt];
-  }
-  __syncthreads();
-  if (row0 < NPAD) {
-    int n = row0 + lane;
-    if (n < N_NODES) {
-      float4 v;
-      v.x = st[wave][0][lane]; v.y = st[wave][1][lane]; v.z = st[wave][2][lane]; v.w = st[wave][3][lane];
-      qi4[n] = v;
-      v.x = st[wave][4][lane]; v.y = st[wave][5][lane]; v.z = st[wave][6][lane]; v.w = st[wave][7][lane];
-      qi4[NPAD + n] = v;
-      v.x = st[wave][8][lane]; v.y = st[wave][9][lane]; v.z = st[wave][10][lane]; v.w = st[wave][11][lane];
-      kj4[n] = v;
-      v.x = st[wave][12][lane]; v.y = st[wave][13][lane]; v.z = st[wave][14][lane]; v.w = st[wave][15][lane];
-      kj4[NPAD + n] = v;
-    }
-  }
-}
-
-__global__ __launch_bounds__(256) void edge_quad_kernel(
-    const int* __restrict__ rowstart, const int* __restrict__ eord,
-    const float4* __restrict__ qi4, const float4* __restrict__ kj4,
-    const unsigned short* __restrict__ xw, unsigned short* __restrict__ aggb,
-    const int* __restrict__ nq, const int* __restrict__ bcnt) {
-  __shared__ volatile float wls[16][4][17];
-  const int t = threadIdx.x;
-  const int wave = t >> 6, lane = t & 63;
-  const int g = lane >> 4, li = lane & 15;
-  const int idx = blockIdx.x * 16 + wave * 4 + g;
-  const int cq = bcnt[0];
-  const bool act = idx < cq;
-  const int n = act ? nq[idx] : 0;
-  const int start = rowstart[n];
-  const int dg = act ? (rowstart[n + 1] - start) : 0;
-  int p = 0;
-  float w0 = 0.f, w1 = 0.f, w2 = 0.f, w3 = 0.f;
-  if (li < dg) {
-    p = eord[start + li];
-    int s = p & 0xffff, r = p >> 16;
-    float4 k4 = kj4[r ? (NPAD + s) : s];
-    float4 q4 = r ? qi4[NPAD + n] : qi4[n];
-    w0 = __expf(fminf(lrelu(q4.x + k4.x), 85.f));
-    w1 = __expf(fminf(lrelu(q4.y + k4.y), 85.f));
-    w2 = __expf(fminf(lrelu(q4.z + k4.z), 85.f));
-    w3 = __expf(fminf(lrelu(q4.w + k4.w), 85.f));
-  }
-  const int wg = (wave << 2) | g;
-  wls[wg][0][li] = w0; wls[wg][1][li] = w1;
-  wls[wg][2][li] = w2; wls[wg][3][li] = w3;
-  float s0 = w0, s1 = w1, s2 = w2, s3 = w3;
-#pragma unroll
-  for (int off = 8; off > 0; off >>= 1) {
-    s0 += __shfl_xor(s0, off); s1 += __shfl_xor(s1, off);
-    s2 += __shfl_xor(s2, off); s3 += __shfl_xor(s3, off);
-  }
-  const int hh = li >> 2;
-  float ssel = hh == 0 ? s0 : hh == 1 ? s1 : hh == 2 ? s2 : s3;
-  float a0 = 0.f, a1 = 0.f, a2 = 0.f, a3 = 0.f, a4 = 0.f, a5 = 0.f, a6 = 0.f, a7 = 0.f;
-  volatile const float* wrh = &wls[wg][hh][0];
-  const int co = li * 8;
-  const int gbase = lane & 48;
-#pragma unroll 1
-  for (int e0 = 0; e0 < dg; e0 += 4) {
-    int pe[4];
-    uint4 v[4];
-#pragma unroll
-    for (int u = 0; u < 4; ++u) {
-      int e = e0 + u;
-      pe[u] = __shfl(p, gbase + (e < dg ? e : 0));
-    }
-#pragma unroll
-    for (int u = 0; u < 4; ++u)
-      v[u] = *(const uint4*)(xw + ((size_t)((pe[u] & 0xffff) + (pe[u] >> 16) * NPAD) << 7) + co);
-#pragma unroll
-    for (int u = 0; u < 4; ++u) {
-      int e = e0 + u;
-      float we = (e < dg) ? wrh[e] : 0.f;
-      a0 = fmaf(lo_f(v[u].x), we, a0); a1 = fmaf(hi_f(v[u].x), we, a1);
-      a2 = fmaf(lo_f(v[u].y), we, a2); a3 = fmaf(hi_f(v[u].y), we, a3);
-      a4 = fmaf(lo_f(v[u].z), we, a4); a5 = fmaf(hi_f(v[u].z), we, a5);
-      a6 = fmaf(lo_f(v[u].w), we, a6); a7 = fmaf(hi_f(v[u].w), we, a7);
-    }
-  }
-  if (act) {
-    float inv = 1.f / (ssel + 1e-16f);
-    uint4 o;
-    o.x = (unsigned)f2bf_bits(a0 * inv) | ((unsigned)f2bf_bits(a1 * inv) << 16);
-    o.y = (unsigned)f2bf_bits(a2 * inv) | ((unsigned)f2bf_bits(a3 * inv) << 16);
-    o.z = (unsigned)f2bf_bits(a4 * inv) | ((unsigned)f2bf_bits(a5 * inv) << 16);
-    o.w = (unsigned)f2bf_bits(a6 * inv) | ((unsigned)f2bf_bits(a7 * inv) << 16);
-    *(uint4*)(aggb + ((size_t)n << 7) + co) = o;
-  }
-}
-
-__global__ __launch_bounds__(256) void edge_big_kernel(
-    const int* __restrict__ rowstart, const int* __restrict__ eord,
-    const float4* __restrict__ qi4, const float4* __restrict__ kj4,
-    const unsigned short* __restrict__ xw, unsigned short* __restrict__ aggb,
-    const int* __restrict__ nw, const int* __restrict__ bcnt) {
-  __shared__ volatile float wls[4][4][72];
-  const int wave = threadIdx.x >> 6, lane = threadIdx.x & 63;
-  const int idx = blockIdx.x * 4 + wave;
-  const int cw = bcnt[1];
-  if (idx >= cw) return;
-  const int n = nw[idx];
-  unsigned* outp = (unsigned*)(aggb + ((size_t)n << 7)) + lane;
-  const int start = rowstart[n];
-  const int deg = rowstart[n + 1] - start;
-  const int hh = lane >> 4;
-  const int ch2 = lane << 1;
-  float2 acc = {0.f, 0.f};
-  float ssel;
-  if (deg <= 64) {
-    int p = 0;
-    float w0 = 0.f, w1 = 0.f, w2 = 0.f, w3 = 0.f;
-    if (lane < deg) {
-      p = eord[start + lane];
-      int s = p & 0xffff, r = p >> 16;
-      float4 k4 = kj4[r ? (NPAD + s) : s];
-      float4 q4 = r ? qi4[NPAD + n] : qi4[n];
-      w0 = __expf(fminf(lrelu(q4.x + k4.x), 85.f));
-      w1 = __expf(fminf(lrelu(q4.y + k4.y), 85.f));
-      w2 = __expf(fminf(lrelu(q4.z + k4.z), 85.f));
-      w3 = __expf(fminf(lrelu(q4.w + k4.w), 85.f));
-    }
-    float s0 = w0, s1 = w1, s2 = w2, s3 = w3;
-#pragma unroll
-    for (int off = 32; off > 0; off >>= 1) {
-      s0 += __shfl_xor(s0, off); s1 += __shfl_xor(s1, off);
-      s2 += __shfl_xor(s2, off); s3 += __shfl_xor(s3, off);
-    }
-    ssel = hh == 0 ? s0 : hh == 1 ? s1 : hh == 2 ? s2 : s3;
-    wls[wave][0][lane] = w0;
-    wls[wave][1][lane] = w1;
-    wls[wave][2][lane] = w2;
-    wls[wave][3][lane] = w3;
-    volatile const float* wrh = &wls[wave][hh][0];
-    const int degp = (deg + 15) & ~15;
-#pragma unroll 1
-    for (int e = 0; e < degp; e += 16) {
-      int pp[16];
-      unsigned vv[16];
-#pragma unroll
-      for (int u = 0; u < 16; ++u)
-        pp[u] = __builtin_amdgcn_readlane(p, e + u);
-#pragma unroll
-      for (int u = 0; u < 16; ++u)
-        vv[u] = *(const unsigned*)(xw + ((size_t)((pp[u] & 0xffff) + (pp[u] >> 16) * NPAD) << 7) + ch2);
-#pragma unroll
-      for (int u = 0; u < 16; ++u) {
-        float we = wrh[e + u];
-        acc.x = fmaf(lo_f(vv[u]), we, acc.x);
-        acc.y = fmaf(hi_f(vv[u]), we, acc.y);
-      }
-    }
-  } else {
-    const float4 q0 = qi4[n], q1 = qi4[NPAD + n];
-    float4 m = make_float4(-1e30f, -1e30f, -1e30f, -1e30f);
-    for (int e = start; e < start + deg; ++e) {
-      int pe = eord[e];
-      int s = pe & 0xffff, r = pe >> 16;
-      float4 k4 = kj4[(size_t)r * NPAD + s];
-      float4 q4 = r ? q1 : q0;
-      m.x = fmaxf(m.x, lrelu(q4.x + k4.x)); m.y = fmaxf(m.y, lrelu(q4.y + k4.y));
-      m.z = fmaxf(m.z, lrelu(q4.z + k4.z)); m.w = fmaxf(m.w, lrelu(q4.w + k4.w));
-    }
-    float4 sv = make_float4(0.f, 0.f, 0.f, 0.f);
-    for (int e = start; e < start + deg; ++e) {
-      int pe = eord[e];
-      int s = pe & 0xffff, r = pe >> 16;
-      float4 k4 = kj4[(size_t)r * NPAD + s];
-      float4 q4 = r ? q1 : q0;
-      float w0 = __expf(lrelu(q4.x + k4.x) - m.x);
-      float w1 = __expf(lrelu(q4.y + k4.y) - m.y);
-      float w2 = __expf(lrelu(q4.z + k4.z) - m.z);
-      float w3 = __expf(lrelu(q4.w + k4.w) - m.w);
-      sv.x += w0; sv.y += w1; sv.z += w2; sv.w += w3;
-      float we = hh == 0 ? w0 : hh == 1 ? w1 : hh == 2 ? w2 : w3;
-      unsigned v = *(const unsigned*)(xw + (((size_t)r * NPAD + s) << 7) + ch2);
-      acc.x = fmaf(lo_f(v), we, acc.x);
-      acc.y = fmaf(hi_f(v), we, acc.y);
-    }
-    ssel = hh == 0 ? sv.x : hh == 1 ? sv.y : hh == 2 ? sv.z : sv.w;
-  }
-  float inv = 1.f / (ssel + 1e-16f);
-  *outp = (unsigned)f2bf_bits(acc.x * inv) | ((unsigned)f2bf_bits(acc.y * inv) << 16);
-}
-
-__global__ __launch_bounds__(64) void prep_proj_kernel(const void* __restrict__ pW0,
-                                                       const void* __restrict__ pW1,
-                                                       const float* __restrict__ cbf,
-                                                       const float* __restrict__ pbf,
-                                                       unsigned short* __restrict__ pWTb2,
-                                                       float* __restrict__ bo2,
-                                                       const int* __restrict__ flags) {
-  int o = blockIdx.x & 127, l = blockIdx.x >> 7, t = threadIdx.x;
-  const void* pWraw = l ? pW1 : pW0;
-  const float* cb = cbf + l * HID;
-  const int f = flags[0];
-  float part = 0.f;
-#pragma unroll
-  for (int i = t; i < HID; i += 64) {
-    float w = f ? ((const float*)pWraw)[o * HID + i] : bf2f(((const unsigned short*)pWraw)[o * HID + i]);
-    pWTb2[(size_t)l * HID * HID + o * HID + i] = f2bf_bits(w);
-    part += cb[i] * w;
-  }
-#pragma unroll
-  for (int off = 32; off > 0; off >>= 1) part += __shfl_xor(part, off);
-  if (t == 0) bo2[l * HID + o] = pbf[l * HID + o] + part;
 }
 
 extern "C" void kernel_launch(void* const* d_in, const int* in_sizes, int n_in,
@@ -679,10 +678,7 @@
   float* bo2 = ws + off; off += 2 * HID;
 
   detect_zero_kernel<<<(2 * NPAD + 16 + 255) / 256, 256, 0, stream>>>((const unsigned short*)x, eidx, flags, deg, 2 * NPAD + 16);
-  cvt_idx_hist_kernel<<<(E_EDGES + 255) / 256, 256, 0, stream>>>(eidx, etype, dstA, pk, deg, flags);
-  bucket_kernel<<<(N_NODES + 255) / 256, 256, 0, stream>>>(deg, bcnt, nq, nwl);
-  cvt_xb_kernel<<<(N_NODES * HID / 8 + 255) / 256, 256, 0, stream>>>(x, hb, N_NODES * HID / 8, flags);
-  cvt_wt_kernel<<<(2 * 2 * HID * HID + 255) / 256, 256, 0, stream>>>(d_in[iW[0]], d_in[iW[1]], Wbt, flags);
+
   {
     P8 tab;
     float* base = ws;
@@ -692,27 +688,26 @@
       tab.src[l * 4 + 2] = d_in[icb[l]]; tab.dstoff[l * 4 + 2] = (int)(cbf - base) + l * HID;         tab.n[l * 4 + 2] = HID;
       tab.src[l * 4 + 3] = d_in[ipb[l]]; tab.dstoff[l * 4 + 3] = (int)(pbf - base) + l * HID;         tab.n[l * 4 + 3] = HID;
     }
-    cvt_params_kernel<<<2, 256, 0, stream>>>(tab, base, flags);
-  }
-
-  scan1_kernel<<<SCAN_B, 256, 0, stream>>>(deg, excl, bsum);
-  scan23_kernel<<<SCAN_B, 256, 0, stream>>>(excl, bsum, rowstart);
+    cvt_all_kernel<<<GB_IDX + GB_XB + GB_WT + 2, 256, 0, stream>>>(eidx, etype, dstA, pk, deg,
+                                                                   x, hb, d_in[iW[0]], d_in[iW[1]], Wbt,
+                                                                   tab, ws, flags);
+  }
+
+  scan1_bucket_kernel<<<SCAN_B + SCAN_B, 256, 0, stream>>>(deg, excl, bsum, bcnt, nq, nwl);
+
+  scan23_prep_kernel<<<SCAN_B + 2 + 64, 256, 0, stream>>>(excl, bsum, rowstart,
+                                                          Wbt, Qf, Kf, qkt_hi, qkt_lo,
+                                                          d_in[ipW[0]], d_in[ipW[1]], cbf, pbf, pWTb2, bo2, flags);
+
   scatter_kernel<<<(E_EDGES + 255) / 256, 256, 0, stream>>>(dstA, pk, rowstart, cnt, eord);
 
-  prep_wq_kernel<<<2, 256, 0, stream>>>(Wbt, Qf, Kf, qkt_hi, qkt_lo);
-  prep_proj_kernel<<<2 * HID, 64, 0, stream>>>(d_in[ipW[0]], d_in[ipW[1]], cbf, pbf, pWTb2, bo2, flags);
-
-  const int RB = NPAD / 64;
-  const int QB = (NPAD + 255) / 256;
   for (int l = 0; l < 2; ++l) {
-    gemm_xw_mfma<<<RB, 256, 0, stream>>>(hb, Wbt + (size_t)l * 2 * HID * HID, xw);
-    qk_mfma_kernel<<<QB, 256, 0, stream>>>(hb, qkt_hi + (size_t)l * 16 * HID, qkt_lo + (size_t)l * 16 * HID,
-                                           (float4*)qi, (float4*)kj);
-    edge_quad_kernel<<<(N_NODES + 15) / 16, 256, 0, stream>>>(rowstart, eord, (const float4*)qi, (const float4*)kj,
-                                                              xw, aggb, nq, bcnt);
-    edge_big_kernel<<<(N_NODES + 3) / 4, 256, 0, stream>>>(rowstart, eord, (const float4*)qi, (const float4*)kj,
-                                                           xw, aggb, nwl, bcnt);
-    proj_mfma<<<RB, 128, 0, stream>>>(aggb, pWTb2 + (size_t)l * HID * HID, bo2 + l * HID, hb,
-                                      (l == 1) ? d_out : nullptr, flags);
-  }
-}
+    gemm_qk_kernel<<<GB_GEMM + GB_QK, 256, 0, stream>>>(hb, Wbt + (size_t)l * 2 * HID * HID, xw,
+                                                        qkt_hi + (size_t)l * 16 * HID, qkt_lo + (size_t)l * 16 * HID,
+                                                        (float4*)qi, (float4*)kj);
+    edge_all_kernel<<<GB_QUAD + GB_BIG, 256, 0, stream>>>(rowstart, eord, (const float4*)qi, (const float4*)kj,
+                                                          xw, aggb, nq, nwl, bcnt);
+    proj_mfma<<<NPAD / 64, 256, 0, stream>>>(aggb, pWTb2 + (size_t)l * HID * HID, bo2 + l * HID, hb,
+                                             (l == 1) ? d_out : nullptr, flags);
+  }
+}
```

After: 343.6 us. 8.2% less time.
